# Optimization experiments

Hardware: AMD Instinct MI355X
Metric: run time of the kernel (lower is better)

The kernel has to match this reference:

```python
import jax, jax.numpy as jnp
import numpy as np

B, SEQ, TOK = 32, 200, 50
E, H, NHID, L = 512, 8, 2048, 6
DH = E // H
VOC, TC_EMB = 12525, 1024

def _make_mask(batch, heads, S):
    # True = masked. Heads 0-5: sliding window of size 10 unmasked.
    # Heads 6+: unmasked only for batch 0 (faithful to original code's indexing).
    # Row 0 (CLS) attends everywhere.
    m = np.ones((batch, heads, S, S), dtype=bool)
    j = np.arange(S)[:, None]
    cols = np.clip(j - 5 + np.arange(10)[None, :], 0, S - 1)
    rows = np.broadcast_to(j, cols.shape)
    local = np.ones((S, S), dtype=bool)
    local[rows.ravel(), cols.ravel()] = False
    m[:, :6] = local
    m[0, 6:] = False
    m[:, :, 0, :] = False
    return jnp.asarray(m)

MASK_101 = _make_mask(B, H, 101)
MASK_200 = _make_mask(B, H, 200)

def _layer_norm(x):
    mu = x.mean(-1, keepdims=True)
    sx = x - mu
    var = (sx * sx).mean(-1, keepdims=True)
    return sx * jax.lax.rsqrt(var + 1e-12)

def _ln_affine(x, g, b):
    return _layer_norm(x) * g + b

def _textcnn(ids, emb, cws, cbs, fw, fb):
    x = emb[ids][:, None, :, :]  # [N,1,50,1024] NCHW
    feats = []
    for w, b in zip(cws, cbs):
        y = jax.lax.conv_general_dilated(x, w, (1, 1), 'VALID',
                dimension_numbers=('NCHW', 'OIHW', 'NCHW'))
        y = jax.nn.relu(y + b[None, :, None, None])[..., 0]  # [N,100,T]
        feats.append(y.max(axis=2))
    return jnp.concatenate(feats, axis=1) @ fw.T + fb  # [N,512]

def _encoder(x, mask, Wq, bq, Wk, bk, Wv, bv, Wo, bo, W1, b1, W2, b2, g1, be1, g2, be2):
    scale = float(np.sqrt(DH))
    def heads(t):  # [B,S,E] -> [B,H,S,DH]
        return t.reshape(t.shape[0], t.shape[1], H, DH).transpose(0, 2, 1, 3)
    for l in range(L):
        q = x @ Wq[l].T + bq[l]
        k = x @ Wk[l].T + bk[l]
        v = x @ Wv[l].T + bv[l]
        scores = jnp.einsum('bhqd,bhkd->bhqk', heads(q), heads(k)) / scale
        attn = jax.nn.softmax(jnp.where(mask, -1e9, scores), axis=-1)
        ctx = jnp.einsum('bhqk,bhkd->bhqd', attn, heads(v))
        ctx = ctx.transpose(0, 2, 1, 3).reshape(x.shape[0], -1, E) @ Wo[l].T + bo[l]
        x = _ln_affine(x + ctx, g1[l], be1[l])
        ff = jax.nn.relu(x @ W1[l].T + b1[l]) @ W2[l].T + b2[l]
        x = _ln_affine(x + ff, g2[l], be2[l])
    return x


def reference(src, label_similarity, tc_emb, cw1, cb1, cw2, cb2, cw3, cb3,
              tc_fc_w, tc_fc_b, Wq, bq, Wk, bk, Wv, bv, Wo, bo,
              W1, b1, W2, b2, ln1_g, ln1_b, ln2_g, ln2_b,
              fc1_w, fc1_b, fc2_w, fc2_b, fc3_w, fc3_b, post_scale, post_bias):
    cws, cbs = (cw1, cw2, cw3), (cb1, cb2, cb3)
    enc = lambda x, m: _encoder(x, m, Wq, bq, Wk, bk, Wv, bv, Wo, bo,
                                W1, b1, W2, b2, ln1_g, ln1_b, ln2_g, ln2_b)

    def post(h, S):
        h = jax.nn.gelu(h @ fc1_w.T + fc1_b, approximate=False)
        h = _layer_norm(h)
        return h * post_scale[:, :S, :] + post_bias[:, :S, :]

    # branch 1: first 100 JDs + CLS
    x = _textcnn(src[:, :100, :].reshape(-1, TOK), tc_emb, cws, cbs, tc_fc_w, tc_fc_b)
    x = _layer_norm(x.reshape(B, 100, E))
    x = jnp.concatenate([jnp.zeros((B, 1, E), x.dtype), x], axis=1)  # [B,101,E]
    pred = post(enc(x, MASK_101), 101)
    pred = pred @ fc2_w.T + fc2_b  # [B,101,200]
    cls_e = pred[:, :1, :]  # [B,1,200]
    tok = pred[:, 1:, :].transpose(0, 2, 1) @ fc3_w.T + fc3_b  # [B,200,200]
    tok = jax.nn.softmax(label_similarity, axis=-1) + 0.4 * tok
    tok = jnp.einsum('bnm,bom->bn', tok, cls_e)  # [B,200]

    # branch 2: all 200 JDs
    y = _textcnn(src.reshape(-1, TOK), tc_emb, cws, cbs, tc_fc_w, tc_fc_b)
    y = _layer_norm(y.reshape(B, SEQ, E))
    all_pred = post(enc(y, MASK_200), SEQ)
    pred1 = all_pred @ fc2_w.T + fc2_b  # [B,200,200]

    nnb = SEQ // 100  # 2
    def seg_soft(t, i):  # faithful (quirky) slice t[:, i:(i+1)*100]
        return jax.nn.softmax(t[:, i:(i + 1) * 100, :].mean(axis=1), axis=-1)
    kl_rows, euc_rows = [], []
    for i in range(nnb):
        kr, er = [], []
        for j in range(nnb):
            c1 = seg_soft(pred1, i) + 1e-6
            c2 = seg_soft(pred1, j) + 1e-6
            a1 = seg_soft(all_pred, i) + 1e-6
            a2 = seg_soft(all_pred, j) + 1e-6
            kr.append((c1 * jnp.log(c1 / c2)).sum(-1))
            er.append(jnp.sqrt(jnp.maximum(((a1 - a2) ** 2).sum(-1), 1e-12)))
        kl_rows.append(jnp.stack(kr, -1))
        euc_rows.append(jnp.stack(er, -1))
    sims_kl = jax.nn.softmax(jnp.stack(kl_rows, 1).reshape(B, -1) * 10, axis=-1) + 1e-6
    sims_euc = jax.nn.softmax(jnp.stack(euc_rows, 1).reshape(B, -1), axis=-1) + 1e-6
    loss = (sims_kl * jnp.log(sims_kl / sims_euc)).sum(-1).mean() * 100000 * 0.2

    return (jax.nn.softmax(tok, axis=-1), jax.nn.softmax(cls_e, axis=-1), loss)


def setup_inputs():
    key = jax.random.key(0)
    ks = jax.random.split(key, 20)
    f = lambda k, s: jax.random.normal(k, s, jnp.float32) * 0.02
    emb = f(ks[0], (VOC, TC_EMB)).at[0].set(0.0)  # padding_idx=0
    return {
        'src': jax.random.randint(ks[1], (B, SEQ, TOK), 0, VOC),
        'label_similarity': jax.random.normal(ks[2], (200, 200), jnp.float32),
        'tc_emb': emb,
        'cw1': f(ks[3], (100, 1, 1, TC_EMB)), 'cb1': jnp.zeros((100,)),
        'cw2': f(ks[4], (100, 1, 2, TC_EMB)), 'cb2': jnp.zeros((100,)),
        'cw3': f(ks[5], (100, 1, 3, TC_EMB)), 'cb3': jnp.zeros((100,)),
        'tc_fc_w': f(ks[6], (E, 300)), 'tc_fc_b': jnp.zeros((E,)),
        'Wq': f(ks[7], (L, E, E)), 'bq': jnp.zeros((L, E)),
        'Wk': f(ks[8], (L, E, E)), 'bk': jnp.zeros((L, E)),
        'Wv': f(ks[9], (L, E, E)), 'bv': jnp.zeros((L, E)),
        'Wo': f(ks[10], (L, E, E)), 'bo': jnp.zeros((L, E)),
        'W1': f(ks[11], (L, NHID, E)), 'b1': jnp.zeros((L, NHID)),
        'W2': f(ks[12], (L, E, NHID)), 'b2': jnp.zeros((L, E)),
        'ln1_g': jnp.ones((L, E)), 'ln1_b': jnp.zeros((L, E)),
        'ln2_g': jnp.ones((L, E)), 'ln2_b': jnp.zeros((L, E)),
        'fc1_w': f(ks[13], (E, E)), 'fc1_b': jnp.zeros((E,)),
        'fc2_w': f(ks[14], (200, E)), 'fc2_b': jnp.zeros((200,)),
        'fc3_w': f(ks[15], (200, 100)), 'fc3_b': jnp.zeros((200,)),
        'post_scale': jnp.ones((B, 300, E)), 'post_bias': jnp.zeros((B, 300, E)),
    }
```

## Files before the change

kernel.cpp:

```cpp
#include <hip/hip_runtime.h>
#include <float.h>
#include <math.h>


#define B_   32
#define SEQ_ 200
#define TOK_ 50
#define E_   512
#define H_   8
#define DH_  64
#define NHID_ 2048
#define L_   6
#define VOC_ 12525
#define TCE_ 1024

typedef unsigned short ushort_t;
typedef __attribute__((ext_vector_type(8))) short bf16x8;
typedef __attribute__((ext_vector_type(4))) float f32x4;
typedef __attribute__((address_space(1))) const unsigned int GU32;
typedef __attribute__((address_space(3))) unsigned int LU32;

__device__ __forceinline__ unsigned short f2bf(float x){
  unsigned u = __float_as_uint(x);
  unsigned r = u + 0x7fff + ((u >> 16) & 1);
  return (unsigned short)(r >> 16);
}
__device__ __forceinline__ float bf2f(unsigned short h){
  return __uint_as_float(((unsigned)h) << 16);
}

__device__ __forceinline__ float waveReduceSum(float v){
#pragma unroll
  for (int o = 32; o > 0; o >>= 1) v += __shfl_down(v, o, 64);
  return v;
}
__device__ __forceinline__ float waveReduceMax(float v){
#pragma unroll
  for (int o = 32; o > 0; o >>= 1) v = fmaxf(v, __shfl_down(v, o, 64));
  return v;
}
__device__ __forceinline__ float blockReduceSum256(float v, float* sm){
  v = waveReduceSum(v);
  int lane = threadIdx.x & 63, w = threadIdx.x >> 6;
  __syncthreads();
  if (lane == 0) sm[w] = v;
  __syncthreads();
  return sm[0] + sm[1] + sm[2] + sm[3];
}
__device__ __forceinline__ float blockReduceMax256(float v, float* sm){
  v = waveReduceMax(v);
  int lane = threadIdx.x & 63, w = threadIdx.x >> 6;
  __syncthreads();
  if (lane == 0) sm[w] = v;
  __syncthreads();
  return fmaxf(fmaxf(sm[0], sm[1]), fmaxf(sm[2], sm[3]));
}

__global__ __launch_bounds__(256) void gemm_k(
    const float* __restrict__ A, const float* __restrict__ B,
    const float* __restrict__ bias, const float* __restrict__ Res,
    float* __restrict__ C,
    int M, int N, int K,
    long long sAm, long long sAk, long long sBn, long long sBk,
    long long sCm, long long sRm,
    int Hd,
    long long bAb, long long bAh, long long bBb, long long bBh,
    long long bCb, long long bCh,
    float alpha, int epi)
{
  __shared__ float As[16][68];
  __shared__ float Bs[16][68];
  int z = blockIdx.z;
  int zb = z / Hd, zh = z - zb * Hd;
  A += (long long)zb * bAb + (long long)zh * bAh;
  B += (long long)zb * bBb + (long long)zh * bBh;
  C += (long long)zb * bCb + (long long)zh * bCh;
  int m0 = blockIdx.y * 64, n0 = blockIdx.x * 64;
  int tid = threadIdx.y * 16 + threadIdx.x;
  float acc[4][4] = {};
  for (int k0 = 0; k0 < K; k0 += 16) {
#pragma unroll
    for (int i = 0; i < 4; ++i) {
      int idx = tid + 256 * i;
      int kk = idx & 15, mm = idx >> 4;
      int m = m0 + mm, k = k0 + kk;
      As[kk][mm] = (m < M && k < K) ? A[(long long)m * sAm + (long long)k * sAk] : 0.f;
      int n = n0 + mm;
      Bs[kk][mm] = (n < N && k < K) ? B[(long long)n * sBn + (long long)k * sBk] : 0.f;
    }
    __syncthreads();
#pragma unroll
    for (int kk = 0; kk < 16; ++kk) {
      float a[4], b[4];
#pragma unroll
      for (int i = 0; i < 4; ++i) a[i] = As[kk][threadIdx.y * 4 + i];
#pragma unroll
      for (int j = 0; j < 4; ++j) b[j] = Bs[kk][threadIdx.x * 4 + j];
#pragma unroll
      for (int i = 0; i < 4; ++i)
#pragma unroll
        for (int j = 0; j < 4; ++j) acc[i][j] = fmaf(a[i], b[j], acc[i][j]);
    }
    __syncthreads();
  }
#pragma unroll
  for (int i = 0; i < 4; ++i) {
    int m = m0 + threadIdx.y * 4 + i;
    if (m >= M) continue;
#pragma unroll
    for (int j = 0; j < 4; ++j) {
      int n = n0 + threadIdx.x * 4 + j;
      if (n >= N) continue;
      float v = acc[i][j] * alpha;
      if (bias) v += bias[n];
      if (epi == 1) v = fmaxf(v, 0.f);
      else if (epi == 2) v = 0.5f * v * (1.f + erff(v * 0.70710678f));
      if (Res) v += Res[(long long)m * sRm + n];
      C[(long long)m * sCm + n] = v;
    }
  }
}

static inline void launch_gemm(hipStream_t st,
    const float* A, const float* B, const float* bias, const float* Res, float* C,
    int M, int N, int K,
    long long sAm, long long sAk, long long sBn, long long sBk,
    long long sCm, long long sRm,
    int nz, int Hd,
    long long bAb, long long bAh, long long bBb, long long bBh,
    long long bCb, long long bCh,
    float alpha, int epi)
{
  dim3 g((N + 63) / 64, (M + 63) / 64, nz), bl(16, 16);
  gemm_k<<<g, bl, 0, st>>>(A, B, bias, Res, C, M, N, K,
                           sAm, sAk, sBn, sBk, sCm, sRm, Hd,
                           bAb, bAh, bBb, bBh, bCb, bCh, alpha, epi);
}

__global__ __launch_bounds__(256) void mgemm_k(
    const ushort_t* __restrict__ Ah, const ushort_t* __restrict__ Al,
    const ushort_t* __restrict__ Bh, const ushort_t* __restrict__ Bl,
    const float* __restrict__ bias, const float* __restrict__ Res,
    float* __restrict__ Cf, ushort_t* __restrict__ Chh, ushort_t* __restrict__ Cll,
    int M, int N, int K, int epi, int Mslice, int Nt, int nsplit,
    int kstepsPer, long long splitStride)
{
  __shared__ __align__(16) ushort_t smem[4][128 * 32];
  int lin = blockIdx.x;
  int xcd = lin & 7;
  int q = lin >> 3;
  int ml = q % Mslice;
  int q2 = q / Mslice;
  int nt = q2 % Nt;
  int sp = q2 / Nt;
  int mt = xcd * Mslice + ml;
  if (mt * 128 >= M) return;
  int m0 = mt * 128, n0 = nt * 128;
  int kbase = sp * kstepsPer;
  int tid = threadIdx.x;
  int lane = tid & 63, wv = tid >> 6;
  int wm = (wv >> 1) * 64, wn = (wv & 1) * 64;
  int fr = lane & 15, fq = lane >> 4;
  f32x4 acc[4][4];
  f32x4 zero = {0.f, 0.f, 0.f, 0.f};
#pragma unroll
  for (int i = 0; i < 4; ++i)
#pragma unroll
    for (int j = 0; j < 4; ++j) acc[i][j] = zero;

  for (int ks = 0; ks < kstepsPer; ++ks) {
    int k0 = (kbase + ks) << 5;
#pragma unroll
    for (int it = 0; it < 8; ++it) {
      int c = tid + it * 256;
      int buf = c >> 9;
      int cc = c & 511;
      int row = cc >> 2, cb = (cc & 3) * 8;
      const ushort_t* gsrc;
      long long grow;
      if (buf < 2) { int ar = m0 + row; if (ar >= M) ar = M - 1; grow = ar;
                     gsrc = buf ? Al : Ah; }
      else         { int br = n0 + row; if (br >= N) br = N - 1; grow = br;
                     gsrc = (buf == 2) ? Bh : Bl; }
      __builtin_amdgcn_global_load_lds((GU32*)(gsrc + grow * K + k0 + cb),
                                       (LU32*)(&smem[buf][0] + cc * 8), 16, 0, 0);
    }
    __syncthreads();
    bf16x8 ah[4], al[4], bh8[4], bl8[4];
#pragma unroll
    for (int i = 0; i < 4; ++i) {
      ah[i]  = *(const bf16x8*)(&smem[0][0] + (wm + i * 16 + fr) * 32 + fq * 8);
      al[i]  = *(const bf16x8*)(&smem[1][0] + (wm + i * 16 + fr) * 32 + fq * 8);
      bh8[i] = *(const bf16x8*)(&smem[2][0] + (wn + i * 16 + fr) * 32 + fq * 8);
      bl8[i] = *(const bf16x8*)(&smem[3][0] + (wn + i * 16 + fr) * 32 + fq * 8);
    }
#pragma unroll
    for (int i = 0; i < 4; ++i)
#pragma unroll
      for (int j = 0; j < 4; ++j) {
        acc[i][j] = __builtin_amdgcn_mfma_f32_16x16x32_bf16(ah[i], bh8[j], acc[i][j], 0, 0, 0);
        acc[i][j] = __builtin_amdgcn_mfma_f32_16x16x32_bf16(ah[i], bl8[j], acc[i][j], 0, 0, 0);
        acc[i][j] = __builtin_amdgcn_mfma_f32_16x16x32_bf16(al[i], bh8[j], acc[i][j], 0, 0, 0);
      }
    __syncthreads();
  }

  if (nsplit > 1) {
    float* Cs = Cf + (long long)sp * splitStride;
#pragma unroll
    for (int i = 0; i < 4; ++i)
#pragma unroll
      for (int j = 0; j < 4; ++j) {
        int col = n0 + wn + j * 16 + fr;
        if (col >= N) continue;
#pragma unroll
        for (int r = 0; r < 4; ++r) {
          int row = m0 + wm + i * 16 + fq * 4 + r;
          if (row >= M) continue;
          Cs[(long long)row * N + col] = acc[i][j][r];
        }
      }
    return;
  }
#pragma unroll
  for (int i = 0; i < 4; ++i) {
#pragma unroll
    for (int j = 0; j < 4; ++j) {
      int col = n0 + wn + j * 16 + fr;
      if (col >= N) continue;
#pragma unroll
      for (int r = 0; r < 4; ++r) {
        int row = m0 + wm + i * 16 + fq * 4 + r;
        if (row >= M) continue;
        float v = acc[i][j][r];
        if (bias) v += bias[col];
        if (epi == 1) v = fmaxf(v, 0.f);
        else if (epi == 2) v = 0.5f * v * (1.f + erff(v * 0.70710678f));
        long long idx = (long long)row * N + col;
        if (Res) v += Res[idx];
        if (Cf) Cf[idx] = v;
        if (Chh) {
          unsigned short h = f2bf(v);
          Chh[idx] = h;
          Cll[idx] = f2bf(v - bf2f(h));
        }
      }
    }
  }
}

__global__ void add_bias2_k(const float* __restrict__ s0, const float* __restrict__ s1,
                            const float* __restrict__ bias, float* __restrict__ o,
                            int total, int N){
  int idx = blockIdx.x * 256 + threadIdx.x;
  if (idx >= total) return;
  o[idx] = s0[idx] + s1[idx] + bias[idx % N];
}

__global__ void qkv_reduce_k(const float* __restrict__ s0, const float* __restrict__ s1,
                             const float* __restrict__ bias, float* __restrict__ o,
                             long long total){
  long long idx = ((long long)blockIdx.x * 256 + threadIdx.x) * 4;
  if (idx >= total) return;
  float4 a = *(const float4*)(s0 + idx);
  float4 b = *(const float4*)(s1 + idx);
  int c = (int)(idx % 1536);
  float4 bi = *(const float4*)(bias + c);
  float4 r;
  r.x = a.x + b.x + bi.x; r.y = a.y + b.y + bi.y;
  r.z = a.z + b.z + bi.z; r.w = a.w + b.w + bi.w;
  *(float4*)(o + idx) = r;
}

#define BND_ROWS 64
#define BND_STAGE 73
__global__ __launch_bounds__(256) void attn_band(
    const float* __restrict__ QKV,
    ushort_t* __restrict__ oh, ushort_t* __restrict__ ol, int S, int nrb)
{
  __shared__ float Kl[BND_STAGE][68];
  __shared__ float Vl[BND_STAGE][68];
  __shared__ float Ql[BND_ROWS][68];
  __shared__ float sc[BND_ROWS][12];
  int bh = blockIdx.x / nrb, rblk = blockIdx.x % nrb;
  int b = bh / 6, h = bh % 6;
  int r0 = 1 + rblk * BND_ROWS;
  int nrows = S - r0; if (nrows > BND_ROWS) nrows = BND_ROWS;
  int lo0 = r0 - 5; if (lo0 < 0) lo0 = 0;
  int hi0 = r0 + nrows - 1 + 4; if (hi0 > S - 1) hi0 = S - 1;
  int cnt = hi0 - lo0 + 1;
  int t = threadIdx.x;
  const float* base = QKV + ((long long)(b * S + lo0)) * 1536 + h * 64;
  for (int idx = t; idx < cnt * 64; idx += 256) {
    int row = idx >> 6, d = idx & 63;
    Kl[row][d] = base[(long long)row * 1536 + 512 + d];
    Vl[row][d] = base[(long long)row * 1536 + 1024 + d];
  }
  const float* qbase = QKV + ((long long)(b * S + r0)) * 1536 + h * 64;
  for (int idx = t; idx < nrows * 64; idx += 256) {
    int row = idx >> 6, d = idx & 63;
    Ql[row][d] = qbase[(long long)row * 1536 + d];
  }
  __syncthreads();
  for (int p = t; p < nrows * 10; p += 256) {
    int ri = p / 10, jo = p - ri * 10;
    int r = r0 + ri;
    int lo = r - 5; if (lo < 0) lo = 0;
    int hi = r + 4; if (hi > S - 1) hi = S - 1;
    int j = lo + jo;
    float s;
    if (j > hi) s = -FLT_MAX;
    else {
      int jl = j - lo0;
      float a = 0.f;
      const float4* qv = (const float4*)&Ql[ri][0];
      const float4* kv = (const float4*)&Kl[jl][0];
#pragma unroll
      for (int c = 0; c < 16; ++c) {
        float4 x = qv[c], y = kv[c];
        a += x.x * y.x + x.y * y.y + x.z * y.z + x.w * y.w;
      }
      s = a * 0.125f;
    }
    sc[ri][jo] = s;
  }
  __syncthreads();
  if (t < nrows) {
    float mx = -FLT_MAX;
#pragma unroll
    for (int jo = 0; jo < 10; ++jo) mx = fmaxf(mx, sc[t][jo]);
    float pv[10]; float sum = 0.f;
#pragma unroll
    for (int jo = 0; jo < 10; ++jo) {
      float s = sc[t][jo];
      float e = (s == -FLT_MAX) ? 0.f : expf(s - mx);
      pv[jo] = e; sum += e;
    }
    float inv = 1.f / sum;
#pragma unroll
    for (int jo = 0; jo < 10; ++jo) sc[t][jo] = pv[jo] * inv;
  }
  __syncthreads();
  for (int idx = t; idx < nrows * 64; idx += 256) {
    int ri = idx >> 6, d = idx & 63;
    int r = r0 + ri;
    int lo = r - 5; if (lo < 0) lo = 0;
    int jbase = lo - lo0;
    float a = 0.f;
#pragma unroll
    for (int jo = 0; jo < 10; ++jo) {
      int jl = jbase + jo; if (jl >= cnt) jl = cnt - 1;
      a += sc[ri][jo] * Vl[jl][d];
    }
    long long o = ((long long)(b * S + r)) * 512 + h * 64 + d;
    unsigned short hh = f2bf(a);
    oh[o] = hh; ol[o] = f2bf(a - bf2f(hh));
  }
}

__global__ __launch_bounds__(256) void attn_full(
    const float* __restrict__ QKV,
    ushort_t* __restrict__ oh, ushort_t* __restrict__ ol, int S)
{
  __shared__ float sm_m[4], sm_l[4], sm_acc[4][64];
  int idx = blockIdx.x;
  int b, h, i;
  if (idx < B_ * H_) { b = idx >> 3; h = idx & 7; i = 0; }
  else { int r = idx - B_ * H_; h = 6 + r / (S - 1); i = 1 + r % (S - 1); b = 0; }
  int t = threadIdx.x, lane = t & 63, w = t >> 6;
  const float* Qr = QKV + ((long long)(b * S + i)) * 1536 + h * 64;
  const float* Kb = QKV + ((long long)(b * S)) * 1536 + 512 + h * 64;
  const float* Vb = QKV + ((long long)(b * S)) * 1536 + 1024 + h * 64;
  float q = Qr[lane];
  float m = -FLT_MAX, l = 0.f, acc = 0.f;
  for (int j0 = w * 4; j0 < S; j0 += 16) {
    float s[4];
#pragma unroll
    for (int c = 0; c < 4; ++c) {
      int j = j0 + c;
      float kv = (j < S) ? Kb[(long long)j * 1536 + lane] : 0.f;
      float r = waveReduceSum(q * kv);
      s[c] = r * 0.125f;
    }
#pragma unroll
    for (int c = 0; c < 4; ++c) {
      s[c] = __shfl(s[c], 0);
      if (j0 + c >= S) s[c] = -FLT_MAX;
    }
    float mc = fmaxf(fmaxf(s[0], s[1]), fmaxf(s[2], s[3]));
    float mn = fmaxf(m, mc);
    float scale = (m == -FLT_MAX) ? 0.f : expf(m - mn);
    float lsum = 0.f, vsum = 0.f;
#pragma unroll
    for (int c = 0; c < 4; ++c) {
      int j = j0 + c;
      if (j < S) {
        float p = expf(s[c] - mn);
        lsum += p;
        vsum += p * Vb[(long long)j * 1536 + lane];
      }
    }
    acc = acc * scale + vsum;
    l = l * scale + lsum;
    m = mn;
  }
  sm_m[w] = m;
  sm_l[w] = l;
  sm_acc[w][lane] = acc;
  __syncthreads();
  if (t < 64) {
    float M = fmaxf(fmaxf(sm_m[0], sm_m[1]), fmaxf(sm_m[2], sm_m[3]));
    float L = 0.f, A = 0.f;
#pragma unroll
    for (int w2 = 0; w2 < 4; ++w2) {
      float e = (sm_m[w2] == -FLT_MAX) ? 0.f : expf(sm_m[w2] - M);
      L += sm_l[w2] * e;
      A += sm_acc[w2][t] * e;
    }
    float ctx = A / L;
    long long o = ((long long)(b * S + i)) * 512 + h * 64 + t;
    unsigned short hh = f2bf(ctx);
    oh[o] = hh; ol[o] = f2bf(ctx - bf2f(hh));
  }
}

__global__ __launch_bounds__(256) void attn_unif(
    const float* __restrict__ QKV,
    ushort_t* __restrict__ oh, ushort_t* __restrict__ ol, int S)
{
  __shared__ float part[4][64];
  __shared__ float vm[64];
  int blk = blockIdx.x;
  int b = 1 + (blk >> 1), h = 6 + (blk & 1);
  int t = threadIdx.x, lane = t & 63, w = t >> 6;
  const float* Vb = QKV + ((long long)(b * S)) * 1536 + 1024 + h * 64;
  float s = 0.f;
  for (int j = w; j < S; j += 4) s += Vb[(long long)j * 1536 + lane];
  part[w][lane] = s;
  __syncthreads();
  if (t < 64) vm[t] = (part[0][t] + part[1][t] + part[2][t] + part[3][t]) * (1.f / S);
  __syncthreads();
  float m = vm[lane];
  unsigned short hh = f2bf(m);
  unsigned short hl = f2bf(m - bf2f(hh));
  for (int i = 1 + w; i < S; i += 4) {
    long long o = ((long long)(b * S + i)) * 512 + h * 64 + lane;
    oh[o] = hh; ol[o] = hl;
  }
}

__global__ void conv_hl(const float* __restrict__ x, ushort_t* __restrict__ h,
                        ushort_t* __restrict__ l, long long n){
  long long i = (long long)blockIdx.x * 256 + threadIdx.x;
  if (i >= n) return;
  float v = x[i];
  unsigned short hh = f2bf(v);
  h[i] = hh;
  l[i] = f2bf(v - bf2f(hh));
}

__global__ void conv_qkv(const float* __restrict__ Wq, const float* __restrict__ Wk,
                         const float* __restrict__ Wv,
                         ushort_t* __restrict__ h, ushort_t* __restrict__ l){
  int idx = blockIdx.x * 256 + threadIdx.x;
  if (idx >= L_ * 1536 * 512) return;
  int li = idx / (1536 * 512);
  int r = (idx / 512) % 1536;
  int c = idx & 511;
  const float* W = (r < 512) ? Wq : (r < 1024) ? Wk : Wv;
  int rr = r & 511;
  float v = W[(long long)li * 262144 + rr * 512 + c];
  unsigned short hh = f2bf(v);
  h[idx] = hh;
  l[idx] = f2bf(v - bf2f(hh));
}

__global__ void pack_bqkv(const float* __restrict__ bq, const float* __restrict__ bk,
                          const float* __restrict__ bv, float* __restrict__ o){
  int idx = blockIdx.x * 256 + threadIdx.x;
  if (idx >= L_ * 1536) return;
  int l = idx / 1536, r = idx % 1536;
  o[idx] = (r < 512) ? bq[l * 512 + r] : (r < 1024) ? bk[l * 512 + r - 512]
                                                    : bv[l * 512 + r - 1024];
}

__global__ void build_tcfw_hl(const float* __restrict__ w,
                              ushort_t* __restrict__ h, ushort_t* __restrict__ l){
  int idx = blockIdx.x * 256 + threadIdx.x;
  if (idx >= 512 * 320) return;
  int r = idx / 320, c = idx - r * 320;
  float v = (c < 300) ? w[r * 300 + c] : 0.f;
  unsigned short hh = f2bf(v);
  h[idx] = hh;
  l[idx] = f2bf(v - bf2f(hh));
}

__global__ void build_wcat(const float* __restrict__ cw1, const float* __restrict__ cw2,
                           const float* __restrict__ cw3, float* __restrict__ w){
  int idx = blockIdx.x * 256 + threadIdx.x;
  if (idx >= 600 * 1024) return;
  int o = idx >> 10, c = idx & 1023;
  float v;
  if      (o < 100) v = cw1[o * 1024 + c];
  else if (o < 200) v = cw2[(o - 100) * 2048 + c];
  else if (o < 300) v = cw2[(o - 200) * 2048 + 1024 + c];
  else if (o < 400) v = cw3[(o - 300) * 3072 + c];
  else if (o < 500) v = cw3[(o - 400) * 3072 + 1024 + c];
  else              v = cw3[(o - 500) * 3072 + 2048 + c];
  w[idx] = v;
}

__global__ void build_wcat_hl(const float* __restrict__ cw1, const float* __restrict__ cw2,
                              const float* __restrict__ cw3,
                              ushort_t* __restrict__ wh, ushort_t* __restrict__ wl){
  int idx = blockIdx.x * 256 + threadIdx.x;
  if (idx >= 640 * 1024) return;
  int o = idx >> 10, c = idx & 1023;
  float v = 0.f;
  if      (o < 100) v = cw1[o * 1024 + c];
  else if (o < 200) v = cw2[(o - 100) * 2048 + c];
  else if (o < 300) v = cw2[(o - 200) * 2048 + 1024 + c];
  else if (o < 400) v = cw3[(o - 300) * 3072 + c];
  else if (o < 500) v = cw3[(o - 400) * 3072 + 1024 + c];
  else if (o < 600) v = cw3[(o - 500) * 3072 + 2048 + c];
  unsigned short h = f2bf(v);
  wh[idx] = h;
  wl[idx] = f2bf(v - bf2f(h));
}

__global__ void feats_k(const float* __restrict__ proj, const int* __restrict__ src,
                        const float* __restrict__ cb1, const float* __restrict__ cb2,
                        const float* __restrict__ cb3, float* __restrict__ feats, int ld){
  __shared__ int ids[TOK_];
  int n = blockIdx.x;
  int t = threadIdx.x;
  if (t < TOK_) ids[t] = src[n * TOK_ + t];
  __syncthreads();
  if (t >= 300) return;
  float bia, m = -FLT_MAX;
  if (t < 100) {
    bia = cb1[t];
    for (int k = 0; k < 50; ++k)
      m = fmaxf(m, proj[(long long)ids[k] * ld + t]);
  } else if (t < 200) {
    int o = t - 100; bia = cb2[o];
    for (int k = 0; k < 49; ++k)
      m = fmaxf(m, proj[(long long)ids[k] * ld + 100 + o] +
                   proj[(long long)ids[k + 1] * ld + 200 + o]);
  } else {
    int o = t - 200; bia = cb3[o];
    for (int k = 0; k < 48; ++k)
      m = fmaxf(m, proj[(long long)ids[k] * ld + 300 + o] +
                   proj[(long long)ids[k + 1] * ld + 400 + o] +
                   proj[(long long)ids[k + 2] * ld + 500 + o]);
  }
  feats[(long long)n * 300 + t] = fmaxf(m + bia, 0.f);
}

__global__ void feats_hl_k(const float* __restrict__ proj, const int* __restrict__ src,
                           const float* __restrict__ cb1, const float* __restrict__ cb2,
                           const float* __restrict__ cb3,
                           ushort_t* __restrict__ fh, ushort_t* __restrict__ fl, int ld){
  __shared__ int ids[TOK_];
  int n = blockIdx.x;
  int t = threadIdx.x;
  if (t < TOK_) ids[t] = src[n * TOK_ + t];
  __syncthreads();
  int region = t >> 7, col = t & 127;
  bool act = col < 100;
  bool pad = (region == 2) && (col >= 100) && (col < 120);
  float a = 0.f;
  if (act) {
    float bia, m = -FLT_MAX;
    if (region == 0) {
      bia = cb1[col];
      for (int k = 0; k < 50; ++k)
        m = fmaxf(m, proj[(long long)ids[k] * ld + col]);
    } else if (region == 1) {
      bia = cb2[col];
      for (int k = 0; k < 49; ++k)
        m = fmaxf(m, proj[(long long)ids[k] * ld + 100 + col] +
                     proj[(long long)ids[k + 1] * ld + 200 + col]);
    } else {
      bia = cb3[col];
      for (int k = 0; k < 48; ++k)
        m = fmaxf(m, proj[(long long)ids[k] * ld + 300 + col] +
                     proj[(long long)ids[k + 1] * ld + 400 + col] +
                     proj[(long long)ids[k + 2] * ld + 500 + col]);
    }
    a = fmaxf(m + bia, 0.f);
  }
  if (act || pad) {
    int outcol = region * 100 + col;
    long long o = (long long)n * 320 + outcol;
    unsigned short hh = f2bf(a);
    fh[o] = hh;
    fl[o] = f2bf(a - bf2f(hh));
  }
}

__global__ __launch_bounds__(256) void ln_k(
    const float* __restrict__ in, long long sstr, int nsplit,
    const float* __restrict__ bias2, const float* __restrict__ res2, int epi2,
    float* __restrict__ out, const float* __restrict__ g, const float* __restrict__ bta,
    ushort_t* __restrict__ oh, ushort_t* __restrict__ ol,
    const float* __restrict__ pscale, const float* __restrict__ pbias, int S)
{
  __shared__ float sm[4];
  long long row = blockIdx.x;
  int t = threadIdx.x;
  const float* x = in + row * E_;
  float v0 = x[t], v1 = x[t + 256];
  for (int s = 1; s < nsplit; ++s) {
    v0 += x[(long long)s * sstr + t];
    v1 += x[(long long)s * sstr + t + 256];
  }
  if (bias2) { v0 += bias2[t]; v1 += bias2[t + 256]; }
  if (epi2 == 1) { v0 = fmaxf(v0, 0.f); v1 = fmaxf(v1, 0.f); }
  else if (epi2 == 2) {
    v0 = 0.5f * v0 * (1.f + erff(v0 * 0.70710678f));
    v1 = 0.5f * v1 * (1.f + erff(v1 * 0.70710678f));
  }
  if (res2) { v0 += res2[row * E_ + t]; v1 += res2[row * E_ + t + 256]; }
  float* y = out + row * E_;
  float mu = blockReduceSum256(v0 + v1, sm) * (1.f / E_);
  float d0 = v0 - mu, d1 = v1 - mu;
  float var = blockReduceSum256(d0 * d0 + d1 * d1, sm) * (1.f / E_);
  float r = rsqrtf(var + 1e-12f);
  float o0 = d0 * r, o1 = d1 * r;
  if (g) { o0 = o0 * g[t] + bta[t]; o1 = o1 * g[t + 256] + bta[t + 256]; }
  if (pscale) {
    long long b = row / S, s = row % S;
    long long off = (b * 300 + s) * E_;
    o0 = o0 * pscale[off + t] + pbias[off + t];
    o1 = o1 * pscale[off + t + 256] + pbias[off + t + 256];
  }
  y[t] = o0; y[t + 256] = o1;
  if (oh) {
    unsigned short h0 = f2bf(o0), h1 = f2bf(o1);
    oh[row * E_ + t] = h0;       oh[row * E_ + t + 256] = h1;
    ol[row * E_ + t] = f2bf(o0 - bf2f(h0));
    ol[row * E_ + t + 256] = f2bf(o1 - bf2f(h1));
  }
}

__global__ void build_x1(const float* __restrict__ xln, float* __restrict__ x1){
  long long idx = (long long)blockIdx.x * 256 + threadIdx.x;
  if (idx >= 3232LL * 512) return;
  long long row = idx >> 9; int c = (int)(idx & 511);
  long long b = row / 101, s = row % 101;
  x1[idx] = (s == 0) ? 0.f : xln[((b * 200) + (s - 1)) * 512 + c];
}

__global__ __launch_bounds__(256) void attn_softmax(float* __restrict__ sc, int S){
  __shared__ float sm[4];
  long long row = blockIdx.x;
  int i = (int)(row % S); long long bh = row / S;
  int h = (int)(bh & 7); int b = (int)(bh >> 3);
  float* p = sc + row * S;
  int t = threadIdx.x;
  bool inr = t < S;
  bool allow;
  if (i == 0) allow = true;
  else if (h < 6) allow = (t >= i - 5) && (t <= i + 4);
  else allow = (b == 0);
  float v = inr ? (allow ? p[t] : -1e9f) : -FLT_MAX;
  float mx = blockReduceMax256(v, sm);
  float e = inr ? expf(v - mx) : 0.f;
  float s = blockReduceSum256(e, sm);
  if (inr) p[t] = e / s;
}

__global__ __launch_bounds__(256) void softmax_rows(const float* __restrict__ in,
                                                    float* __restrict__ out, int n){
  __shared__ float sm[4];
  long long row = blockIdx.x;
  const float* x = in + row * n;
  float* y = out + row * n;
  int t = threadIdx.x;
  float v0 = (t < n) ? x[t] : -FLT_MAX;
  float v1 = (t + 256 < n) ? x[t + 256] : -FLT_MAX;
  float mx = blockReduceMax256(fmaxf(v0, v1), sm);
  float e0 = (t < n) ? expf(v0 - mx) : 0.f;
  float e1 = (t + 256 < n) ? expf(v1 - mx) : 0.f;
  float s = blockReduceSum256(e0 + e1, sm);
  if (t < n) y[t] = e0 / s;
  if (t + 256 < n) y[t + 256] = e1 / s;
}

__global__ void copy_cls(const float* __restrict__ pred, float* __restrict__ cls){
  int idx = blockIdx.x * 256 + threadIdx.x;
  if (idx >= B_ * 200) return;
  int b = idx / 200, m = idx % 200;
  cls[idx] = pred[(long long)b * 101 * 200 + m];
}

__global__ __launch_bounds__(256) void tokvec_k(const float* __restrict__ lsoft,
                         const float* __restrict__ tokmat,
                         const float* __restrict__ cls, float* __restrict__ tv){
  __shared__ float sm[4];
  int bn = blockIdx.x; int b = bn / 200, n = bn % 200;
  int t = threadIdx.x;
  float s = 0.f;
  if (t < 200)
    s = (lsoft[n * 200 + t] + 0.4f * tokmat[((long long)b * 200 + n) * 200 + t]) * cls[b * 200 + t];
  float tot = blockReduceSum256(s, sm);
  if (t == 0) tv[bn] = tot;
}

__global__ __launch_bounds__(256) void seg_soft_k(const float* __restrict__ pred,
                         const float* __restrict__ allp,
                         float* __restrict__ c0, float* __restrict__ c1,
                         float* __restrict__ a0, float* __restrict__ a1){
  __shared__ float sm[4];
  int b = blockIdx.x, which = blockIdx.y;
  const float* srcp; int C;
  if (which < 2) { srcp = pred; C = 200; } else { srcp = allp; C = 512; }
  int i = which & 1;
  int start = i, cnt = i ? 199 : 100;
  float* dst = (which == 0) ? c0 : (which == 1) ? c1 : (which == 2) ? a0 : a1;
  const float* base = srcp + ((long long)b * 200 + start) * C;
  int t = threadIdx.x;
  float m0 = 0.f, m1 = 0.f;
  for (int r = 0; r < cnt; ++r) {
    if (t < C)       m0 += base[(long long)r * C + t];
    if (t + 256 < C) m1 += base[(long long)r * C + t + 256];
  }
  float inv = 1.f / cnt;
  m0 *= inv; m1 *= inv;
  float v0 = (t < C) ? m0 : -FLT_MAX;
  float v1 = (t + 256 < C) ? m1 : -FLT_MAX;
  float mx = blockReduceMax256(fmaxf(v0, v1), sm);
  float e0 = (t < C) ? expf(v0 - mx) : 0.f;
  float e1 = (t + 256 < C) ? expf(v1 - mx) : 0.f;
  float s = blockReduceSum256(e0 + e1, sm);
  if (t < C)       dst[(long long)b * C + t] = e0 / s;
  if (t + 256 < C) dst[(long long)b * C + t + 256] = e1 / s;
}

__global__ __launch_bounds__(256) void loss_partial_k(const float* __restrict__ c0,
                         const float* __restrict__ c1,
                         const float* __restrict__ a0, const float* __restrict__ a1,
                         float* __restrict__ partial){
  __shared__ float sm[4];
  int b = blockIdx.x, t = threadIdx.x;
  float k01 = 0.f, k10 = 0.f;
  if (t < 200) {
    float x = c0[b * 200 + t] + 1e-6f, y = c1[b * 200 + t] + 1e-6f;
    k01 = x * logf(x / y);
    k10 = y * logf(y / x);
  }
  float K01 = blockReduceSum256(k01, sm);
  float K10 = blockReduceSum256(k10, sm);
  float d0 = a0[b * 512 + t] - a1[b * 512 + t];
  float d1 = a0[b * 512 + t + 256] - a1[b * 512 + t + 256];
  float E2 = blockReduceSum256(d0 * d0 + d1 * d1, sm);
  if (t == 0) {
    float euc = sqrtf(fmaxf(E2, 1e-12f));
    float kv[4] = {0.f, K01 * 10.f, K10 * 10.f, 0.f};
    float ev[4] = {1e-6f, euc, euc, 1e-6f};
    float mk = fmaxf(fmaxf(kv[0], kv[1]), fmaxf(kv[2], kv[3]));
    float me = fmaxf(fmaxf(ev[0], ev[1]), fmaxf(ev[2], ev[3]));
    float sk = 0.f, se = 0.f;
    for (int q = 0; q < 4; ++q) { kv[q] = expf(kv[q] - mk); sk += kv[q];
                                  ev[q] = expf(ev[q] - me); se += ev[q]; }
    float p = 0.f;
    for (int q = 0; q < 4; ++q) {
      float aa = kv[q] / sk + 1e-6f, bb = ev[q] / se + 1e-6f;
      p += aa * logf(aa / bb);
    }
    partial[b] = p;
  }
}

__global__ void loss_final_k(const float* __restrict__ partial, float* __restrict__ out){
  if (threadIdx.x == 0) {
    float s = 0.f;
    for (int b = 0; b < B_; ++b) s += partial[b];
    out[0] = s * (100000.f * 0.2f / B_);
  }
}

extern "C" void kernel_launch(void* const* d_in, const int* in_sizes, int n_in,
                              void* d_out, int out_size, void* d_ws, size_t ws_size,
                              hipStream_t stream) {
  const int*   src   = (const int*)  d_in[0];
  const float* lab   = (const float*)d_in[1];
  const float* emb   = (const float*)d_in[2];
  const float* cw1   = (const float*)d_in[3];
  const float* cb1   = (const float*)d_in[4];
  const float* cw2   = (const float*)d_in[5];
  const float* cb2   = (const float*)d_in[6];
  const float* cw3   = (const float*)d_in[7];
  const float* cb3   = (const float*)d_in[8];
  const float* tcfw  = (const float*)d_in[9];
  const float* tcfb  = (const float*)d_in[10];
  const float* Wq    = (const float*)d_in[11];
  const float* bq    = (const float*)d_in[12];
  const float* Wk    = (const float*)d_in[13];
  const float* bk    = (const float*)d_in[14];
  const float* Wv    = (const float*)d_in[15];
  const float* bv    = (const float*)d_in[16];
  const float* Wo    = (const float*)d_in[17];
  const float* bo    = (const float*)d_in[18];
  const float* W1    = (const float*)d_in[19];
  const float* b1v   = (const float*)d_in[20];
  const float* W2    = (const float*)d_in[21];
  const float* b2v   = (const float*)d_in[22];
  const float* g1    = (const float*)d_in[23];
  const float* be1   = (const float*)d_in[24];
  const float* g2    = (const float*)d_in[25];
  const float* be2   = (const float*)d_in[26];
  const float* fc1w  = (const float*)d_in[27];
  const float* fc1b  = (const float*)d_in[28];
  const float* fc2w  = (const float*)d_in[29];
  const float* fc2b  = (const float*)d_in[30];
  const float* fc3w  = (const float*)d_in[31];
  const float* fc3b  = (const float*)d_in[32];
  const float* pscale= (const float*)d_in[33];
  const float* pbias = (const float*)d_in[34];
  float* out = (float*)d_out;
  float* ws  = (float*)d_ws;
  ushort_t* wsu = (ushort_t*)d_ws;

  const size_t NEED_MFMA = 215200000ULL;

  if (ws_size >= NEED_MFMA) {
    const long long P_EMBH  = 0;
    const long long P_EMBL  = 6412800;
    const long long P_WCATH = 12825600;
    const long long P_WCATL = 13153280;
    const long long P_PROJ  = 13480960;
    const long long P_FEATS = 21496960;
    const long long SZW4 = 6LL * 512 * 512;
    const long long SZW1 = 6LL * 2048 * 512;
    const long long UQKVH = 0;
    const long long UQKVL = 3 * SZW4;
    const long long UOH = 6 * SZW4, UOL = 7 * SZW4;
    const long long U1H = 8 * SZW4,            U1L = 8 * SZW4 + SZW1;
    const long long U2H = 8 * SZW4 + 2 * SZW1, U2L = 8 * SZW4 + 3 * SZW1;
    const long long UF1H = 8 * SZW4 + 4 * SZW1, UF1L = UF1H + 262144;
    const long long O_BIG  = 19136512;
    const long long O_XLN  = 32243712;
    const long long O_X1   = 35520512;
    const long long O_QKV  = 37175296;
    const long long O_TMP  = 47005696;
    const long long O_XH   = 50282496;
    const long long O_XL   = 51920896;
    const long long O_SM   = 53559296;
    const long long O_LSOFT= O_SM;
    const long long O_CLS  = O_LSOFT + 40000;
    const long long O_TV   = O_CLS + 6400;
    const long long O_C0   = O_TV + 6400;
    const long long O_C1   = O_C0 + 6400;
    const long long O_A0   = O_C1 + 6400;
    const long long O_A1   = O_A0 + 16384;
    const long long O_PART = O_A1 + 16384;
    const long long O_BQKV = O_PART + 64;
    const long long O_FC2W = O_BQKV + 9216;

    ushort_t* EMBH = (ushort_t*)(ws + P_EMBH);
    ushort_t* EMBL = (ushort_t*)(ws + P_EMBL);
    ushort_t* WCATH= (ushort_t*)(ws + P_WCATH);
    ushort_t* WCATL= (ushort_t*)(ws + P_WCATL);
    float* PROJ = ws + P_PROJ;
    ushort_t* FH = (ushort_t*)(ws + P_FEATS);
    ushort_t* FL = FH + 6400LL * 320;
    float* BIG  = ws + O_BIG;
    float* XLN  = ws + O_XLN;
    float* X1   = ws + O_X1;
    float* QKV  = ws + O_QKV;
    float* TMP  = ws + O_TMP;
    ushort_t* TCFWH = (ushort_t*)(ws + O_TMP);
    ushort_t* TCFWL = TCFWH + 512 * 320;
    ushort_t* XH = (ushort_t*)(ws + O_XH);
    ushort_t* XL = (ushort_t*)(ws + O_XL);
    float* LSOFT= ws + O_LSOFT;
    float* CLS  = ws + O_CLS;
    float* TV   = ws + O_TV;
    float* C0p  = ws + O_C0;
    float* C1p  = ws + O_C1;
    float* A0p  = ws + O_A0;
    float* A1p  = ws + O_A1;
    float* PART = ws + O_PART;
    float* BQKV = ws + O_BQKV;
    ushort_t* FC2WH = (ushort_t*)(ws + O_FC2W);
    ushort_t* FC2WL = FC2WH + 200 * 512;
    float* SPLIT = QKV;
    float* ALLP  = TMP;
    float* PRED  = QKV;
    float* FC2S  = QKV + 6553600;
    float* TOKMAT= QKV + 3276800;
    const long long QKV_SPLIT_STRIDE = O_BIG - O_QKV;

    auto mgemm = [&](const ushort_t* Ah, const ushort_t* Al,
                     const ushort_t* Bh, const ushort_t* Bl,
                     const float* bias, const float* Res, float* Cf,
                     ushort_t* Ch, ushort_t* Cl, int M, int N, int K, int epi,
                     int nsplit, long long splitStride){
      int Mt = (M + 127) / 128;
      int Nt = (N + 127) / 128;
      int Mslice = (Mt + 7) / 8;
      int kst = (K / nsplit) >> 5;
      dim3 g(8 * Mslice * Nt * nsplit);
      mgemm_k<<<g, 256, 0, stream>>>(Ah, Al, Bh, Bl, bias, Res, Cf, Ch, Cl,
                                     M, N, K, epi, Mslice, Nt, nsplit, kst, splitStride);
    };

    conv_hl<<<(VOC_ * TCE_ + 255) / 256, 256, 0, stream>>>(emb, EMBH, EMBL, (long long)VOC_ * TCE_);
    build_wcat_hl<<<(640 * 1024 + 255) / 256, 256, 0, stream>>>(cw1, cw2, cw3, WCATH, WCATL);
    mgemm(EMBH, EMBL, WCATH, WCATL, nullptr, nullptr, PROJ, nullptr, nullptr,
          VOC_, 640, TCE_, 0, 1, 0);
    feats_hl_k<<<B_ * SEQ_, 384, 0, stream>>>(PROJ, src, cb1, cb2, cb3, FH, FL, 640);
    build_tcfw_hl<<<(512 * 320 + 255) / 256, 256, 0, stream>>>(tcfw, TCFWH, TCFWL);
    mgemm(FH, FL, TCFWH, TCFWL, nullptr, nullptr, SPLIT, nullptr, nullptr,
          B_ * SEQ_, E_, 320, 0, 2, 6400LL * 512);
    ln_k<<<B_ * SEQ_, 256, 0, stream>>>(SPLIT, 6400LL * 512, 2, tcfb, nullptr, 0,
                                        XLN, nullptr, nullptr, nullptr, nullptr,
                                        nullptr, nullptr, SEQ_);
    build_x1<<<(3232 * 512 + 255) / 256, 256, 0, stream>>>(XLN, X1);

    conv_qkv<<<(L_ * 1536 * 512 + 255) / 256, 256, 0, stream>>>(Wq, Wk, Wv,
                                                                wsu + UQKVH, wsu + UQKVL);
    pack_bqkv<<<(L_ * 1536 + 255) / 256, 256, 0, stream>>>(bq, bk, bv, BQKV);
    conv_hl<<<(int)((SZW4 + 255) / 256), 256, 0, stream>>>(Wo, wsu + UOH, wsu + UOL, SZW4);
    conv_hl<<<(int)((SZW1 + 255) / 256), 256, 0, stream>>>(W1, wsu + U1H, wsu + U1L, SZW1);
    conv_hl<<<(int)((SZW1 + 255) / 256), 256, 0, stream>>>(W2, wsu + U2H, wsu + U2L, SZW1);
    conv_hl<<<(262144 + 255) / 256, 256, 0, stream>>>(fc1w, wsu + UF1H, wsu + UF1L, 262144);
    conv_hl<<<(200 * 512 + 255) / 256, 256, 0, stream>>>(fc2w, FC2WH, FC2WL, 200 * 512);

    auto encoder = [&](float* X, int S, int R){
      ushort_t* BIGH = (ushort_t*)BIG;
      ushort_t* BIGL = BIGH + (long long)R * NHID_;
      int nrb = (S - 1 + BND_ROWS - 1) / BND_ROWS;
      int nfull = B_ * H_ + 2 * (S - 1);
      long long sstr = (long long)R * E_;
      long long qtotal = (long long)R * 1536;
      for (int l = 0; l < L_; ++l) {
        long long oq = (long long)l * 1536 * 512;
        long long o4 = (long long)l * E_ * E_;
        long long o1 = (long long)l * NHID_ * E_;
        const float* bo_l = bo + l * E_;
        const float* b1_l = b1v + l * NHID_; const float* b2_l = b2v + l * E_;
        const float* g1_l = g1 + l * E_;  const float* be1_l = be1 + l * E_;
        const float* g2_l = g2 + l * E_;  const float* be2_l = be2 + l * E_;

        mgemm(XH, XL, wsu + UQKVH + oq, wsu + UQKVL + oq, nullptr,
              nullptr, QKV, nullptr, nullptr, R, 1536, E_, 0, 2, QKV_SPLIT_STRIDE);
        qkv_reduce_k<<<(int)((qtotal / 4 + 255) / 256), 256, 0, stream>>>(
            QKV, BIG, BQKV + l * 1536, QKV, qtotal);
        attn_band<<<B_ * 6 * nrb, 256, 0, stream>>>(QKV, XH, XL, S, nrb);
        attn_full<<<nfull, 256, 0, stream>>>(QKV, XH, XL, S);
        attn_unif<<<(B_ - 1) * 2, 256, 0, stream>>>(QKV, XH, XL, S);
        mgemm(XH, XL, wsu + UOH + o4, wsu + UOL + o4, nullptr, nullptr,
              SPLIT, nullptr, nullptr, R, E_, E_, 0, 4, sstr);
        ln_k<<<R, 256, 0, stream>>>(SPLIT, sstr, 4, bo_l, X, 0,
                                    X, g1_l, be1_l, XH, XL, nullptr, nullptr, S);
        mgemm(XH, XL, wsu + U1H + o1, wsu + U1L + o1, b1_l, nullptr, nullptr,
              BIGH, BIGL, R, NHID_, E_, 1 , 1, 0);
        mgemm(BIGH, BIGL, wsu + U2H + o1, wsu + U2L + o1, nullptr, nullptr,
              SPLIT, nullptr, nullptr, R, E_, NHID_, 0, 4, sstr);
        ln_k<<<R, 256, 0, stream>>>(SPLIT, sstr, 4, b2_l, X, 0,
                                    X, g2_l, be2_l, XH, XL, nullptr, nullptr, S);
      }
    };

    auto post = [&](int S, int R){
      long long sstr = (long long)R * E_;
      mgemm(XH, XL, wsu + UF1H, wsu + UF1L, nullptr, nullptr,
            SPLIT, nullptr, nullptr, R, E_, E_, 0, 4, sstr);
      ln_k<<<R, 256, 0, stream>>>(SPLIT, sstr, 4, fc1b, nullptr, 2 ,
                                  ALLP, nullptr, nullptr, XH, XL, pscale, pbias, S);
      mgemm(XH, XL, FC2WH, FC2WL, nullptr, nullptr, FC2S,
            nullptr, nullptr, R, 200, E_, 0, 2, (long long)R * 200);
      add_bias2_k<<<(R * 200 + 255) / 256, 256, 0, stream>>>(
          FC2S, FC2S + (long long)R * 200, fc2b, PRED, R * 200, 200);
    };

    conv_hl<<<((3232 * 512) + 255) / 256, 256, 0, stream>>>(X1, XH, XL, 3232LL * 512);
    encoder(X1, 101, B_ * 101);
    post(101, B_ * 101);
    copy_cls<<<(B_ * 200 + 255) / 256, 256, 0, stream>>>(PRED, CLS);
    softmax_rows<<<B_, 256, 0, stream>>>(CLS, out + 6400, 200);
    softmax_rows<<<200, 256, 0, stream>>>(lab, LSOFT, 200);
    launch_gemm(stream, PRED + 200, fc3w, fc3b, nullptr, TOKMAT, 200, 200, 100,
                1, 200, 100, 1, 200, 0,
                B_, 1, 101LL * 200, 0, 0, 0, 200LL * 200, 0, 1.f, 0);
    tokvec_k<<<B_ * 200, 256, 0, stream>>>(LSOFT, TOKMAT, CLS, TV);
    softmax_rows<<<B_, 256, 0, stream>>>(TV, out, 200);

    conv_hl<<<((6400 * 512) + 255) / 256, 256, 0, stream>>>(XLN, XH, XL, 6400LL * 512);
    encoder(XLN, SEQ_, B_ * SEQ_);
    post(SEQ_, B_ * SEQ_);
    {
      dim3 g(B_, 4);
      seg_soft_k<<<g, 256, 0, stream>>>(PRED, ALLP, C0p, C1p, A0p, A1p);
    }
    loss_partial_k<<<B_, 256, 0, stream>>>(C0p, C1p, A0p, A1p, PART);
    loss_final_k<<<1, 64, 0, stream>>>(PART, out + 12800);
    return;
  }

  const long long O_WCAT = 0;
  const long long O_PROJ = 614400;
  const long long O_FEATS= 8129400;
  const long long O_BIG  = 0;
  const long long O_XLN  = 13107200;
  const long long O_X1   = 16384000;
  const long long O_XQ   = 18038784;
  const long long O_XK   = 21315584;
  const long long O_XV   = 24592384;
  const long long O_CTX  = 27869184;
  const long long O_TMP  = 31145984;
  const long long O_SM   = 34422784;
  const long long O_LSOFT= O_SM;
  const long long O_CLS  = O_LSOFT + 40000;
  const long long O_TV   = O_CLS + 6400;
  const long long O_C0   = O_TV + 6400;
  const long long O_C1   = O_C0 + 6400;
  const long long O_A0   = O_C1 + 6400;
  const long long O_A1   = O_A0 + 16384;
  const long long O_PART = O_A1 + 16384;

  float* WCAT = ws + O_WCAT;
  float* PROJ = ws + O_PROJ;
  float* FEATS= ws + O_FEATS;
  float* BIG  = ws + O_BIG;
  float* XLN  = ws + O_XLN;
  float* X1   = ws + O_X1;
  float* XQ   = ws + O_XQ;
  float* XK   = ws + O_XK;
  float* XV   = ws + O_XV;
  float* CTX  = ws + O_CTX;
  float* TMP  = ws + O_TMP;
  float* LSOFT= ws + O_LSOFT;
  float* CLS  = ws + O_CLS;
  float* TV   = ws + O_TV;
  float* C0p  = ws + O_C0;
  float* C1p  = ws + O_C1;
  float* A0p  = ws + O_A0;
  float* A1p  = ws + O_A1;
  float* PART = ws + O_PART;

  build_wcat<<<(600 * 1024 + 255) / 256, 256, 0, stream>>>(cw1, cw2, cw3, WCAT);
  launch_gemm(stream, emb, WCAT, nullptr, nullptr, PROJ,
              VOC_, 600, TCE_, TCE_, 1, TCE_, 1, 600, 0,
              1, 1, 0,0,0,0,0,0, 1.f, 0);
  feats_k<<<B_ * SEQ_, 320, 0, stream>>>(PROJ, src, cb1, cb2, cb3, FEATS, 600);
  launch_gemm(stream, FEATS, tcfw, tcfb, nullptr, XLN,
              B_ * SEQ_, E_, 300, 300, 1, 300, 1, E_, 0,
              1, 1, 0,0,0,0,0,0, 1.f, 0);
  ln_k<<<B_ * SEQ_, 256, 0, stream>>>(XLN, 0, 1, nullptr, nullptr, 0,
                                      XLN, nullptr, nullptr, nullptr, nullptr,
                                      nullptr, nullptr, SEQ_);
  build_x1<<<(3232 * 512 + 255) / 256, 256, 0, stream>>>(XLN, X1);

  auto encoder = [&](float* X, int S, int R){
    for (int l = 0; l < L_; ++l) {
      const float* Wq_l = Wq + (long long)l * E_ * E_;
      const float* Wk_l = Wk + (long long)l * E_ * E_;
      const float* Wv_l = Wv + (long long)l * E_ * E_;
      const float* Wo_l = Wo + (long long)l * E_ * E_;
      const float* W1_l = W1 + (long long)l * NHID_ * E_;
      const float* W2_l = W2 + (long long)l * E_ * NHID_;
      const float* bq_l = bq + l * E_;  const float* bk_l = bk + l * E_;
      const float* bv_l = bv + l * E_;  const float* bo_l = bo + l * E_;
      const float* b1_l = b1v + l * NHID_; const float* b2_l = b2v + l * E_;
      const float* g1_l = g1 + l * E_;  const float* be1_l = be1 + l * E_;
      const float* g2_l = g2 + l * E_;  const float* be2_l = be2 + l * E_;

      launch_gemm(stream, X, Wq_l, bq_l, nullptr, XQ, R, E_, E_,
                  E_, 1, E_, 1, E_, 0, 1, 1, 0,0,0,0,0,0, 1.f, 0);
      launch_gemm(stream, X, Wk_l, bk_l, nullptr, XK, R, E_, E_,
                  E_, 1, E_, 1, E_, 0, 1, 1, 0,0,0,0,0,0, 1.f, 0);
      launch_gemm(stream, X, Wv_l, bv_l, nullptr, XV, R, E_, E_,
                  E_, 1, E_, 1, E_, 0, 1, 1, 0,0,0,0,0,0, 1.f, 0);
      launch_gemm(stream, XQ, XK, nullptr, nullptr, BIG, S, S, DH_,
                  E_, 1, E_, 1, S, 0,
                  B_ * H_, H_,
                  (long long)S * E_, DH_, (long long)S * E_, DH_,
                  (long long)H_ * S * S, (long long)S * S,
                  0.125f, 0);
      attn_softmax<<<B_ * H_ * S, 256, 0, stream>>>(BIG, S);
      launch_gemm(stream, BIG, XV, nullptr, nullptr, CTX, S, DH_, S,
                  S, 1, 1, E_, E_, 0,
                  B_ * H_, H_,
                  (long long)H_ * S * S, (long long)S * S,
                  (long long)S * E_, DH_,
                  (long long)S * E_, DH_,
                  1.f, 0);
      launch_gemm(stream, CTX, Wo_l, bo_l, X, TMP, R, E_, E_,
                  E_, 1, E_, 1, E_, E_, 1, 1, 0,0,0,0,0,0, 1.f, 0);
      ln_k<<<R, 256, 0, stream>>>(TMP, 0, 1, nullptr, nullptr, 0,
                                  X, g1_l, be1_l, nullptr, nullptr, nullptr, nullptr, S);
      launch_gemm(stream, X, W1_l, b1_l, nullptr, BIG, R, NHID_, E_,
                  E_, 1, E_, 1, NHID_, 0, 1, 1, 0,0,0,0,0,0, 1.f, 1);
      launch_gemm(stream, BIG, W2_l, b2_l, X, TMP, R, E_, NHID_,
                  NHID_, 1, NHID_, 1, E_, E_, 1, 1, 0,0,0,0,0,0, 1.f, 0);
      ln_k<<<R, 256, 0, stream>>>(TMP, 0, 1, nullptr, nullptr, 0,
                                  X, g2_l, be2_l, nullptr, nullptr, nullptr, nullptr, S);
    }
  };

  auto post = [&](float* X, int S, int R, float* H1v, float* ALLPf, float* PREDf){
    launch_gemm(stream, X, fc1w, fc1b, nullptr, H1v, R, E_, E_,
                E_, 1, E_, 1, E_, 0, 1, 1, 0,0,0,0,0,0, 1.f, 2);
    ln_k<<<R, 256, 0, stream>>>(H1v, 0, 1, nullptr, nullptr, 0,
                                ALLPf, nullptr, nullptr, nullptr, nullptr, pscale, pbias, S);
    launch_gemm(stream, ALLPf, fc2w, fc2b, nullptr, PREDf, R, 200, E_,
                E_, 1, E_, 1, 200, 0, 1, 1, 0,0,0,0,0,0, 1.f, 0);
  };

  encoder(X1, 101, B_ * 101);
  post(X1, 101, B_ * 101, XQ, XK, CTX);
  copy_cls<<<(B_ * 200 + 255) / 256, 256, 0, stream>>>(CTX, CLS);
  softmax_rows<<<B_, 256, 0, stream>>>(CLS, out + 6400, 200);
  softmax_rows<<<200, 256, 0, stream>>>(lab, LSOFT, 200);
  launch_gemm(stream, CTX + 200, fc3w, fc3b, nullptr, TMP, 200, 200, 100,
              1, 200, 100, 1, 200, 0,
              B_, 1, 101LL * 200, 0, 0, 0, 200LL * 200, 0, 1.f, 0);
  tokvec_k<<<B_ * 200, 256, 0, stream>>>(LSOFT, TMP, CLS, TV);
  softmax_rows<<<B_, 256, 0, stream>>>(TV, out, 200);

  encoder(XLN, SEQ_, B_ * SEQ_);
  post(XLN, SEQ_, B_ * SEQ_, XQ, XK, CTX);
  {
    dim3 g(B_, 4);
    seg_soft_k<<<g, 256, 0, stream>>>(CTX, XK, C0p, C1p, A0p, A1p);
  }
  loss_partial_k<<<B_, 256, 0, stream>>>(C0p, C1p, A0p, A1p, PART);
  loss_final_k<<<1, 64, 0, stream>>>(PART, out + 12800);
}
```

Baseline: 3.918 ms.

## Batch both encoder passes into one concatenated row stack sharing GEMMs

Concatenates the 101-token and 200-token sequences into one 9632-row activation buffer so each encoder layer runs its QKV, output, FFN and post-projection GEMMs once over both passes instead of twice. Attention kernels get a row offset so each sequence length is still handled separately. The QKV bias is fused into the GEMM epilogue, which drops the split-K reduce kernel. The FFN is split into two 1024-wide halves with accumulate-into-output split-K, which lets the workspace be repacked. The goal is fewer launches and better GPU fill on the smaller pass. The cost is a larger working set and in-place build_x1 aliasing.

```diff
diff --git a/kernel.cpp b/kernel.cpp
--- a/kernel.cpp
+++ b/kernel.cpp
@@ -13,6 +13,9 @@
 #define L_   6
 #define VOC_ 12525
 #define TCE_ 1024
+#define R1_  3232
+#define R2_  6400
+#define R3_  9632
 
 typedef unsigned short ushort_t;
 typedef __attribute__((ext_vector_type(8))) short bf16x8;
@@ -142,8 +145,8 @@
     const ushort_t* __restrict__ Bh, const ushort_t* __restrict__ Bl,
     const float* __restrict__ bias, const float* __restrict__ Res,
     float* __restrict__ Cf, ushort_t* __restrict__ Chh, ushort_t* __restrict__ Cll,
-    int M, int N, int K, int epi, int Mslice, int Nt, int nsplit,
-    int kstepsPer, long long splitStride)
+    int M, int N, int K, int ldB, int epi, int Mslice, int Nt, int nsplit,
+    int kstepsPer, long long splitStride, int accum)
 {
   __shared__ __align__(16) ushort_t smem[4][128 * 32];
   int lin = blockIdx.x;
@@ -177,12 +180,12 @@
       int cc = c & 511;
       int row = cc >> 2, cb = (cc & 3) * 8;
       const ushort_t* gsrc;
-      long long grow;
-      if (buf < 2) { int ar = m0 + row; if (ar >= M) ar = M - 1; grow = ar;
-                     gsrc = buf ? Al : Ah; }
-      else         { int br = n0 + row; if (br >= N) br = N - 1; grow = br;
-                     gsrc = (buf == 2) ? Bh : Bl; }
-      __builtin_amdgcn_global_load_lds((GU32*)(gsrc + grow * K + k0 + cb),
+      long long gaddr;
+      if (buf < 2) { int ar = m0 + row; if (ar >= M) ar = M - 1;
+                     gsrc = buf ? Al : Ah; gaddr = (long long)ar * K + k0 + cb; }
+      else         { int br = n0 + row; if (br >= N) br = N - 1;
+                     gsrc = (buf == 2) ? Bh : Bl; gaddr = (long long)br * ldB + k0 + cb; }
+      __builtin_amdgcn_global_load_lds((GU32*)(gsrc + gaddr),
                                        (LU32*)(&smem[buf][0] + cc * 8), 16, 0, 0);
     }
     __syncthreads();
@@ -217,7 +220,9 @@
         for (int r = 0; r < 4; ++r) {
           int row = m0 + wm + i * 16 + fq * 4 + r;
           if (row >= M) continue;
-          Cs[(long long)row * N + col] = acc[i][j][r];
+          long long idx = (long long)row * N + col;
+          if (accum) Cs[idx] += acc[i][j][r];
+          else       Cs[idx]  = acc[i][j][r];
         }
       }
     return;
@@ -257,26 +262,11 @@
   o[idx] = s0[idx] + s1[idx] + bias[idx % N];
 }
 
-__global__ void qkv_reduce_k(const float* __restrict__ s0, const float* __restrict__ s1,
-                             const float* __restrict__ bias, float* __restrict__ o,
-                             long long total){
-  long long idx = ((long long)blockIdx.x * 256 + threadIdx.x) * 4;
-  if (idx >= total) return;
-  float4 a = *(const float4*)(s0 + idx);
-  float4 b = *(const float4*)(s1 + idx);
-  int c = (int)(idx % 1536);
-  float4 bi = *(const float4*)(bias + c);
-  float4 r;
-  r.x = a.x + b.x + bi.x; r.y = a.y + b.y + bi.y;
-  r.z = a.z + b.z + bi.z; r.w = a.w + b.w + bi.w;
-  *(float4*)(o + idx) = r;
-}
-
 #define BND_ROWS 64
 #define BND_STAGE 73
 __global__ __launch_bounds__(256) void attn_band(
     const float* __restrict__ QKV,
-    ushort_t* __restrict__ oh, ushort_t* __restrict__ ol, int S, int nrb)
+    ushort_t* __restrict__ oh, ushort_t* __restrict__ ol, int S, int nrb, int row0)
 {
   __shared__ float Kl[BND_STAGE][68];
   __shared__ float Vl[BND_STAGE][68];
@@ -290,13 +280,13 @@
   int hi0 = r0 + nrows - 1 + 4; if (hi0 > S - 1) hi0 = S - 1;
   int cnt = hi0 - lo0 + 1;
   int t = threadIdx.x;
-  const float* base = QKV + ((long long)(b * S + lo0)) * 1536 + h * 64;
+  const float* base = QKV + ((long long)(row0 + b * S + lo0)) * 1536 + h * 64;
   for (int idx = t; idx < cnt * 64; idx += 256) {
     int row = idx >> 6, d = idx & 63;
     Kl[row][d] = base[(long long)row * 1536 + 512 + d];
     Vl[row][d] = base[(long long)row * 1536 + 1024 + d];
   }
-  const float* qbase = QKV + ((long long)(b * S + r0)) * 1536 + h * 64;
+  const float* qbase = QKV + ((long long)(row0 + b * S + r0)) * 1536 + h * 64;
   for (int idx = t; idx < nrows * 64; idx += 256) {
     int row = idx >> 6, d = idx & 63;
     Ql[row][d] = qbase[(long long)row * 1536 + d];
@@ -352,7 +342,7 @@
       int jl = jbase + jo; if (jl >= cnt) jl = cnt - 1;
       a += sc[ri][jo] * Vl[jl][d];
     }
-    long long o = ((long long)(b * S + r)) * 512 + h * 64 + d;
+    long long o = ((long long)(row0 + b * S + r)) * 512 + h * 64 + d;
     unsigned short hh = f2bf(a);
     oh[o] = hh; ol[o] = f2bf(a - bf2f(hh));
   }
@@ -360,7 +350,7 @@
 
 __global__ __launch_bounds__(256) void attn_full(
     const float* __restrict__ QKV,
-    ushort_t* __restrict__ oh, ushort_t* __restrict__ ol, int S)
+    ushort_t* __restrict__ oh, ushort_t* __restrict__ ol, int S, int row0)
 {
   __shared__ float sm_m[4], sm_l[4], sm_acc[4][64];
   int idx = blockIdx.x;
@@ -368,9 +358,9 @@
   if (idx < B_ * H_) { b = idx >> 3; h = idx & 7; i = 0; }
   else { int r = idx - B_ * H_; h = 6 + r / (S - 1); i = 1 + r % (S - 1); b = 0; }
   int t = threadIdx.x, lane = t & 63, w = t >> 6;
-  const float* Qr = QKV + ((long long)(b * S + i)) * 1536 + h * 64;
-  const float* Kb = QKV + ((long long)(b * S)) * 1536 + 512 + h * 64;
-  const float* Vb = QKV + ((long long)(b * S)) * 1536 + 1024 + h * 64;
+  const float* Qr = QKV + ((long long)(row0 + b * S + i)) * 1536 + h * 64;
+  const float* Kb = QKV + ((long long)(row0 + b * S)) * 1536 + 512 + h * 64;
+  const float* Vb = QKV + ((long long)(row0 + b * S)) * 1536 + 1024 + h * 64;
   float q = Qr[lane];
   float m = -FLT_MAX, l = 0.f, acc = 0.f;
   for (int j0 = w * 4; j0 < S; j0 += 16) {
@@ -418,7 +408,7 @@
       A += sm_acc[w2][t] * e;
     }
     float ctx = A / L;
-    long long o = ((long long)(b * S + i)) * 512 + h * 64 + t;
+    long long o = ((long long)(row0 + b * S + i)) * 512 + h * 64 + t;
     unsigned short hh = f2bf(ctx);
     oh[o] = hh; ol[o] = f2bf(ctx - bf2f(hh));
   }
@@ -426,14 +416,14 @@
 
 __global__ __launch_bounds__(256) void attn_unif(
     const float* __restrict__ QKV,
-    ushort_t* __restrict__ oh, ushort_t* __restrict__ ol, int S)
+    ushort_t* __restrict__ oh, ushort_t* __restrict__ ol, int S, int row0)
 {
   __shared__ float part[4][64];
   __shared__ float vm[64];
   int blk = blockIdx.x;
   int b = 1 + (blk >> 1), h = 6 + (blk & 1);
   int t = threadIdx.x, lane = t & 63, w = t >> 6;
-  const float* Vb = QKV + ((long long)(b * S)) * 1536 + 1024 + h * 64;
+  const float* Vb = QKV + ((long long)(row0 + b * S)) * 1536 + 1024 + h * 64;
   float s = 0.f;
   for (int j = w; j < S; j += 4) s += Vb[(long long)j * 1536 + lane];
   part[w][lane] = s;
@@ -444,7 +434,7 @@
   unsigned short hh = f2bf(m);
   unsigned short hl = f2bf(m - bf2f(hh));
   for (int i = 1 + w; i < S; i += 4) {
-    long long o = ((long long)(b * S + i)) * 512 + h * 64 + lane;
+    long long o = ((long long)(row0 + b * S + i)) * 512 + h * 64 + lane;
     oh[o] = hh; ol[o] = hl;
   }
 }
@@ -604,7 +594,8 @@
     const float* __restrict__ bias2, const float* __restrict__ res2, int epi2,
     float* __restrict__ out, const float* __restrict__ g, const float* __restrict__ bta,
     ushort_t* __restrict__ oh, ushort_t* __restrict__ ol,
-    const float* __restrict__ pscale, const float* __restrict__ pbias, int S)
+    const float* __restrict__ pscale, const float* __restrict__ pbias,
+    int S, long long bnd)
 {
   __shared__ float sm[4];
   long long row = blockIdx.x;
@@ -630,7 +621,11 @@
   float o0 = d0 * r, o1 = d1 * r;
   if (g) { o0 = o0 * g[t] + bta[t]; o1 = o1 * g[t + 256] + bta[t + 256]; }
   if (pscale) {
-    long long b = row / S, s = row % S;
+    long long b, s;
+    if (bnd >= 0) {
+      if (row < bnd) { b = row / 101; s = row % 101; }
+      else { long long rr = row - bnd; b = rr / 200; s = rr % 200; }
+    } else { b = row / S; s = row % S; }
     long long off = (b * 300 + s) * E_;
     o0 = o0 * pscale[off + t] + pbias[off + t];
     o1 = o1 * pscale[off + t + 256] + pbias[off + t + 256];
@@ -644,12 +639,12 @@
   }
 }
 
-__global__ void build_x1(const float* __restrict__ xln, float* __restrict__ x1){
+__global__ void build_x1(float* __restrict__ xc){
   long long idx = (long long)blockIdx.x * 256 + threadIdx.x;
-  if (idx >= 3232LL * 512) return;
+  if (idx >= (long long)R1_ * 512) return;
   long long row = idx >> 9; int c = (int)(idx & 511);
   long long b = row / 101, s = row % 101;
-  x1[idx] = (s == 0) ? 0.f : xln[((b * 200) + (s - 1)) * 512 + c];
+  xc[idx] = (s == 0) ? 0.f : xc[((long long)R1_ + b * 200 + (s - 1)) * 512 + c];
 }
 
 __global__ __launch_bounds__(256) void attn_softmax(float* __restrict__ sc, int S){
@@ -823,15 +818,9 @@
   float* ws  = (float*)d_ws;
   ushort_t* wsu = (ushort_t*)d_ws;
 
-  const size_t NEED_MFMA = 215200000ULL;
-
-  if (ws_size >= NEED_MFMA) {
-    const long long P_EMBH  = 0;
-    const long long P_EMBL  = 6412800;
-    const long long P_WCATH = 12825600;
-    const long long P_WCATL = 13153280;
-    const long long P_PROJ  = 13480960;
-    const long long P_FEATS = 21496960;
+  const size_t NEED_COMB = 215100000ULL;
+
+  if (ws_size >= NEED_COMB) {
     const long long SZW4 = 6LL * 512 * 512;
     const long long SZW1 = 6LL * 2048 * 512;
     const long long UQKVH = 0;
@@ -840,85 +829,73 @@
     const long long U1H = 8 * SZW4,            U1L = 8 * SZW4 + SZW1;
     const long long U2H = 8 * SZW4 + 2 * SZW1, U2L = 8 * SZW4 + 3 * SZW1;
     const long long UF1H = 8 * SZW4 + 4 * SZW1, UF1L = UF1H + 262144;
-    const long long O_BIG  = 19136512;
-    const long long O_XLN  = 32243712;
-    const long long O_X1   = 35520512;
-    const long long O_QKV  = 37175296;
-    const long long O_TMP  = 47005696;
-    const long long O_XH   = 50282496;
-    const long long O_XL   = 51920896;
-    const long long O_SM   = 53559296;
-    const long long O_LSOFT= O_SM;
-    const long long O_CLS  = O_LSOFT + 40000;
-    const long long O_TV   = O_CLS + 6400;
-    const long long O_C0   = O_TV + 6400;
-    const long long O_C1   = O_C0 + 6400;
-    const long long O_A0   = O_C1 + 6400;
-    const long long O_A1   = O_A0 + 16384;
-    const long long O_PART = O_A1 + 16384;
-    const long long O_BQKV = O_PART + 64;
-    const long long O_FC2W = O_BQKV + 9216;
-
-    ushort_t* EMBH = (ushort_t*)(ws + P_EMBH);
-    ushort_t* EMBL = (ushort_t*)(ws + P_EMBL);
-    ushort_t* WCATH= (ushort_t*)(ws + P_WCATH);
-    ushort_t* WCATL= (ushort_t*)(ws + P_WCATL);
-    float* PROJ = ws + P_PROJ;
-    ushort_t* FH = (ushort_t*)(ws + P_FEATS);
+    const long long O_W    = 0;
+    const long long O_QKV  = 19136512;
+    const long long O_BIG  = 33931264;
+    const long long O_XC   = 43794432;
+    const long long O_XHL  = 48726016;
+    const long long O_BQKV = 53657600;
+    const long long O_FC2W = 53666816;
+    ushort_t* EMBH = (ushort_t*)(ws + O_QKV);
+    ushort_t* EMBL = EMBH + (long long)VOC_ * TCE_;
+    ushort_t* WCATH= (ushort_t*)(ws + O_BIG);
+    ushort_t* WCATL= WCATH + 640 * 1024;
+    float* PROJ  = ws + O_BIG + 655360;
+    ushort_t* FH = (ushort_t*)(ws + O_QKV);
     ushort_t* FL = FH + 6400LL * 320;
-    float* BIG  = ws + O_BIG;
-    float* XLN  = ws + O_XLN;
-    float* X1   = ws + O_X1;
+    ushort_t* TCFWH = (ushort_t*)(ws + O_QKV + 2048000);
+    ushort_t* TCFWL = TCFWH + 512 * 320;
+    float* XALLS = ws + O_QKV + 2211840;
     float* QKV  = ws + O_QKV;
-    float* TMP  = ws + O_TMP;
-    ushort_t* TCFWH = (ushort_t*)(ws + O_TMP);
-    ushort_t* TCFWL = TCFWH + 512 * 320;
-    ushort_t* XH = (ushort_t*)(ws + O_XH);
-    ushort_t* XL = (ushort_t*)(ws + O_XL);
-    float* LSOFT= ws + O_LSOFT;
-    float* CLS  = ws + O_CLS;
-    float* TV   = ws + O_TV;
-    float* C0p  = ws + O_C0;
-    float* C1p  = ws + O_C1;
-    float* A0p  = ws + O_A0;
-    float* A1p  = ws + O_A1;
-    float* PART = ws + O_PART;
+    float* SPLIT= ws + O_QKV;
+    float* XC   = ws + O_XC;
+    ushort_t* XH = (ushort_t*)(ws + O_XHL);
+    ushort_t* XL = XH + (long long)R3_ * 512;
+    ushort_t* BIGH = (ushort_t*)(ws + O_BIG);
+    ushort_t* BIGL = BIGH + (long long)R3_ * 1024;
+    float* ALLP = ws + O_BIG;
     float* BQKV = ws + O_BQKV;
     ushort_t* FC2WH = (ushort_t*)(ws + O_FC2W);
     ushort_t* FC2WL = FC2WH + 200 * 512;
-    float* SPLIT = QKV;
-    float* ALLP  = TMP;
-    float* PRED  = QKV;
-    float* FC2S  = QKV + 6553600;
-    float* TOKMAT= QKV + 3276800;
-    const long long QKV_SPLIT_STRIDE = O_BIG - O_QKV;
+    float* FC2S  = ws + O_QKV + 9863168;
+    float* PRED  = ws + O_QKV;
+    float* TOKMAT= ws + O_QKV + 1926400;
+    float* CLS   = ws + O_QKV + 3206400;
+    float* TV    = ws + O_QKV + 3212800;
+    float* LSOFT = ws + O_QKV + 3219200;
+    float* C0p   = ws + O_QKV + 3259200;
+    float* C1p   = ws + O_QKV + 3265600;
+    float* A0p   = ws + O_QKV + 3272000;
+    float* A1p   = ws + O_QKV + 3288384;
+    float* PART  = ws + O_QKV + 3304768;
 
     auto mgemm = [&](const ushort_t* Ah, const ushort_t* Al,
-                     const ushort_t* Bh, const ushort_t* Bl,
+                     const ushort_t* Bh, const ushort_t* Bl, int ldB,
                      const float* bias, const float* Res, float* Cf,
                      ushort_t* Ch, ushort_t* Cl, int M, int N, int K, int epi,
-                     int nsplit, long long splitStride){
+                     int nsplit, long long splitStride, int accum){
       int Mt = (M + 127) / 128;
       int Nt = (N + 127) / 128;
       int Mslice = (Mt + 7) / 8;
       int kst = (K / nsplit) >> 5;
       dim3 g(8 * Mslice * Nt * nsplit);
       mgemm_k<<<g, 256, 0, stream>>>(Ah, Al, Bh, Bl, bias, Res, Cf, Ch, Cl,
-                                     M, N, K, epi, Mslice, Nt, nsplit, kst, splitStride);
+                                     M, N, K, ldB, epi, Mslice, Nt, nsplit,
+                                     kst, splitStride, accum);
     };
 
     conv_hl<<<(VOC_ * TCE_ + 255) / 256, 256, 0, stream>>>(emb, EMBH, EMBL, (long long)VOC_ * TCE_);
     build_wcat_hl<<<(640 * 1024 + 255) / 256, 256, 0, stream>>>(cw1, cw2, cw3, WCATH, WCATL);
-    mgemm(EMBH, EMBL, WCATH, WCATL, nullptr, nullptr, PROJ, nullptr, nullptr,
-          VOC_, 640, TCE_, 0, 1, 0);
+    mgemm(EMBH, EMBL, WCATH, WCATL, TCE_, nullptr, nullptr, PROJ, nullptr, nullptr,
+          VOC_, 640, TCE_, 0, 1, 0, 0);
     feats_hl_k<<<B_ * SEQ_, 384, 0, stream>>>(PROJ, src, cb1, cb2, cb3, FH, FL, 640);
     build_tcfw_hl<<<(512 * 320 + 255) / 256, 256, 0, stream>>>(tcfw, TCFWH, TCFWL);
-    mgemm(FH, FL, TCFWH, TCFWL, nullptr, nullptr, SPLIT, nullptr, nullptr,
-          B_ * SEQ_, E_, 320, 0, 2, 6400LL * 512);
-    ln_k<<<B_ * SEQ_, 256, 0, stream>>>(SPLIT, 6400LL * 512, 2, tcfb, nullptr, 0,
-                                        XLN, nullptr, nullptr, nullptr, nullptr,
-                                        nullptr, nullptr, SEQ_);
-    build_x1<<<(3232 * 512 + 255) / 256, 256, 0, stream>>>(XLN, X1);
+    mgemm(FH, FL, TCFWH, TCFWL, 320, nullptr, nullptr, XALLS, nullptr, nullptr,
+          R2_, E_, 320, 0, 2, 3276800LL, 0);
+    ln_k<<<R2_, 256, 0, stream>>>(XALLS, 3276800LL, 2, tcfb, nullptr, 0,
+                                  XC + (long long)R1_ * 512, nullptr, nullptr,
+                                  nullptr, nullptr, nullptr, nullptr, SEQ_, -1);
+    build_x1<<<(int)(((long long)R1_ * 512 + 255) / 256), 256, 0, stream>>>(XC);
 
     conv_qkv<<<(L_ * 1536 * 512 + 255) / 256, 256, 0, stream>>>(Wq, Wk, Wv,
                                                                 wsu + UQKVH, wsu + UQKVL);
@@ -929,57 +906,58 @@
     conv_hl<<<(262144 + 255) / 256, 256, 0, stream>>>(fc1w, wsu + UF1H, wsu + UF1L, 262144);
     conv_hl<<<(200 * 512 + 255) / 256, 256, 0, stream>>>(fc2w, FC2WH, FC2WL, 200 * 512);
 
-    auto encoder = [&](float* X, int S, int R){
-      ushort_t* BIGH = (ushort_t*)BIG;
-      ushort_t* BIGL = BIGH + (long long)R * NHID_;
-      int nrb = (S - 1 + BND_ROWS - 1) / BND_ROWS;
-      int nfull = B_ * H_ + 2 * (S - 1);
-      long long sstr = (long long)R * E_;
-      long long qtotal = (long long)R * 1536;
-      for (int l = 0; l < L_; ++l) {
-        long long oq = (long long)l * 1536 * 512;
-        long long o4 = (long long)l * E_ * E_;
-        long long o1 = (long long)l * NHID_ * E_;
-        const float* bo_l = bo + l * E_;
-        const float* b1_l = b1v + l * NHID_; const float* b2_l = b2v + l * E_;
-        const float* g1_l = g1 + l * E_;  const float* be1_l = be1 + l * E_;
-        const float* g2_l = g2 + l * E_;  const float* be2_l = be2 + l * E_;
-
-        mgemm(XH, XL, wsu + UQKVH + oq, wsu + UQKVL + oq, nullptr,
-              nullptr, QKV, nullptr, nullptr, R, 1536, E_, 0, 2, QKV_SPLIT_STRIDE);
-        qkv_reduce_k<<<(int)((qtotal / 4 + 255) / 256), 256, 0, stream>>>(
-            QKV, BIG, BQKV + l * 1536, QKV, qtotal);
-        attn_band<<<B_ * 6 * nrb, 256, 0, stream>>>(QKV, XH, XL, S, nrb);
-        attn_full<<<nfull, 256, 0, stream>>>(QKV, XH, XL, S);
-        attn_unif<<<(B_ - 1) * 2, 256, 0, stream>>>(QKV, XH, XL, S);
-        mgemm(XH, XL, wsu + UOH + o4, wsu + UOL + o4, nullptr, nullptr,
-              SPLIT, nullptr, nullptr, R, E_, E_, 0, 4, sstr);
-        ln_k<<<R, 256, 0, stream>>>(SPLIT, sstr, 4, bo_l, X, 0,
-                                    X, g1_l, be1_l, XH, XL, nullptr, nullptr, S);
-        mgemm(XH, XL, wsu + U1H + o1, wsu + U1L + o1, b1_l, nullptr, nullptr,
-              BIGH, BIGL, R, NHID_, E_, 1 , 1, 0);
-        mgemm(BIGH, BIGL, wsu + U2H + o1, wsu + U2L + o1, nullptr, nullptr,
-              SPLIT, nullptr, nullptr, R, E_, NHID_, 0, 4, sstr);
-        ln_k<<<R, 256, 0, stream>>>(SPLIT, sstr, 4, b2_l, X, 0,
-                                    X, g2_l, be2_l, XH, XL, nullptr, nullptr, S);
+    conv_hl<<<(int)(((long long)R3_ * 512 + 255) / 256), 256, 0, stream>>>(
+        XC, XH, XL, (long long)R3_ * 512);
+
+    const long long sstr = (long long)R3_ * 512;
+    const int nrb1 = (101 - 1 + BND_ROWS - 1) / BND_ROWS;
+    const int nrb2 = (200 - 1 + BND_ROWS - 1) / BND_ROWS;
+    const int nfull1 = B_ * H_ + 2 * (101 - 1);
+    const int nfull2 = B_ * H_ + 2 * (200 - 1);
+    for (int l = 0; l < L_; ++l) {
+      long long oq = (long long)l * 1536 * 512;
+      long long o4 = (long long)l * E_ * E_;
+      long long o1 = (long long)l * NHID_ * E_;
+      const float* bo_l = bo + l * E_;
+      const float* b1_l = b1v + l * NHID_; const float* b2_l = b2v + l * E_;
+      const float* g1_l = g1 + l * E_;  const float* be1_l = be1 + l * E_;
+      const float* g2_l = g2 + l * E_;  const float* be2_l = be2 + l * E_;
+
+      mgemm(XH, XL, wsu + UQKVH + oq, wsu + UQKVL + oq, 512, BQKV + l * 1536,
+            nullptr, QKV, nullptr, nullptr, R3_, 1536, E_, 0, 1, 0, 0);
+      attn_band<<<B_ * 6 * nrb1, 256, 0, stream>>>(QKV, XH, XL, 101, nrb1, 0);
+      attn_full<<<nfull1, 256, 0, stream>>>(QKV, XH, XL, 101, 0);
+      attn_unif<<<(B_ - 1) * 2, 256, 0, stream>>>(QKV, XH, XL, 101, 0);
+      attn_band<<<B_ * 6 * nrb2, 256, 0, stream>>>(QKV, XH, XL, 200, nrb2, R1_);
+      attn_full<<<nfull2, 256, 0, stream>>>(QKV, XH, XL, 200, R1_);
+      attn_unif<<<(B_ - 1) * 2, 256, 0, stream>>>(QKV, XH, XL, 200, R1_);
+      mgemm(XH, XL, wsu + UOH + o4, wsu + UOL + o4, 512, nullptr, nullptr,
+            SPLIT, nullptr, nullptr, R3_, E_, E_, 0, 2, sstr, 0);
+      ln_k<<<R3_, 256, 0, stream>>>(SPLIT, sstr, 2, bo_l, XC, 0,
+                                    XC, g1_l, be1_l, XH, XL, nullptr, nullptr, 0, -1);
+      for (int h = 0; h < 2; ++h) {
+        mgemm(XH, XL, wsu + U1H + o1 + (long long)h * 1024 * 512,
+              wsu + U1L + o1 + (long long)h * 1024 * 512, 512,
+              b1_l + h * 1024, nullptr, nullptr, BIGH, BIGL,
+              R3_, 1024, E_, 1 , 1, 0, 0);
+        mgemm(BIGH, BIGL, wsu + U2H + o1 + h * 1024,
+              wsu + U2L + o1 + h * 1024, 2048, nullptr, nullptr,
+              SPLIT, nullptr, nullptr, R3_, E_, 1024, 0, 2, sstr, h);
       }
-    };
-
-    auto post = [&](int S, int R){
-      long long sstr = (long long)R * E_;
-      mgemm(XH, XL, wsu + UF1H, wsu + UF1L, nullptr, nullptr,
-            SPLIT, nullptr, nullptr, R, E_, E_, 0, 4, sstr);
-      ln_k<<<R, 256, 0, stream>>>(SPLIT, sstr, 4, fc1b, nullptr, 2 ,
-                                  ALLP, nullptr, nullptr, XH, XL, pscale, pbias, S);
-      mgemm(XH, XL, FC2WH, FC2WL, nullptr, nullptr, FC2S,
-            nullptr, nullptr, R, 200, E_, 0, 2, (long long)R * 200);
-      add_bias2_k<<<(R * 200 + 255) / 256, 256, 0, stream>>>(
-          FC2S, FC2S + (long long)R * 200, fc2b, PRED, R * 200, 200);
-    };
-
-    conv_hl<<<((3232 * 512) + 255) / 256, 256, 0, stream>>>(X1, XH, XL, 3232LL * 512);
-    encoder(X1, 101, B_ * 101);
-    post(101, B_ * 101);
+      ln_k<<<R3_, 256, 0, stream>>>(SPLIT, sstr, 2, b2_l, XC, 0,
+                                    XC, g2_l, be2_l, XH, XL, nullptr, nullptr, 0, -1);
+    }
+
+    mgemm(XH, XL, wsu + UF1H, wsu + UF1L, 512, nullptr, nullptr,
+          SPLIT, nullptr, nullptr, R3_, E_, E_, 0, 2, sstr, 0);
+    ln_k<<<R3_, 256, 0, stream>>>(SPLIT, sstr, 2, fc1b, nullptr, 2 ,
+                                  ALLP, nullptr, nullptr, XH, XL,
+                                  pscale, pbias, 0, (long long)R1_);
+    mgemm(XH, XL, FC2WH, FC2WL, 512, nullptr, nullptr, FC2S,
+          nullptr, nullptr, R3_, 200, E_, 0, 2, (long long)R3_ * 200, 0);
+    add_bias2_k<<<(R3_ * 200 + 255) / 256, 256, 0, stream>>>(
+        FC2S, FC2S + (long long)R3_ * 200, fc2b, PRED, R3_ * 200, 200);
+
     copy_cls<<<(B_ * 200 + 255) / 256, 256, 0, stream>>>(PRED, CLS);
     softmax_rows<<<B_, 256, 0, stream>>>(CLS, out + 6400, 200);
     softmax_rows<<<200, 256, 0, stream>>>(lab, LSOFT, 200);
@@ -988,13 +966,11 @@
                 B_, 1, 101LL * 200, 0, 0, 0, 200LL * 200, 0, 1.f, 0);
     tokvec_k<<<B_ * 200, 256, 0, stream>>>(LSOFT, TOKMAT, CLS, TV);
     softmax_rows<<<B_, 256, 0, stream>>>(TV, out, 200);
-
-    conv_hl<<<((6400 * 512) + 255) / 256, 256, 0, stream>>>(XLN, XH, XL, 6400LL * 512);
-    encoder(XLN, SEQ_, B_ * SEQ_);
-    post(SEQ_, B_ * SEQ_);
     {
       dim3 g(B_, 4);
-      seg_soft_k<<<g, 256, 0, stream>>>(PRED, ALLP, C0p, C1p, A0p, A1p);
+      seg_soft_k<<<g, 256, 0, stream>>>(PRED + (long long)R1_ * 200,
+                                        ALLP + (long long)R1_ * 512,
+                                        C0p, C1p, A0p, A1p);
     }
     loss_partial_k<<<B_, 256, 0, stream>>>(C0p, C1p, A0p, A1p, PART);
     loss_final_k<<<1, 64, 0, stream>>>(PART, out + 12800);
@@ -1004,7 +980,7 @@
   const long long O_WCAT = 0;
   const long long O_PROJ = 614400;
   const long long O_FEATS= 8129400;
-  const long long O_BIG  = 0;
+  const long long O_BIGf = 0;
   const long long O_XLN  = 13107200;
   const long long O_X1   = 16384000;
   const long long O_XQ   = 18038784;
@@ -1025,7 +1001,7 @@
   float* WCAT = ws + O_WCAT;
   float* PROJ = ws + O_PROJ;
   float* FEATS= ws + O_FEATS;
-  float* BIG  = ws + O_BIG;
+  float* BIG  = ws + O_BIGf;
   float* XLN  = ws + O_XLN;
   float* X1   = ws + O_X1;
   float* XQ   = ws + O_XQ;
@@ -1052,8 +1028,13 @@
               1, 1, 0,0,0,0,0,0, 1.f, 0);
   ln_k<<<B_ * SEQ_, 256, 0, stream>>>(XLN, 0, 1, nullptr, nullptr, 0,
                                       XLN, nullptr, nullptr, nullptr, nullptr,
-                                      nullptr, nullptr, SEQ_);
-  build_x1<<<(3232 * 512 + 255) / 256, 256, 0, stream>>>(XLN, X1);
+                                      nullptr, nullptr, SEQ_, -1);
+  {
+  }
+  {
+  }
+  extern __global__ void build_x1_sep(const float*, float*);
+  build_x1_sep<<<(int)((3232LL * 512 + 255) / 256), 256, 0, stream>>>(XLN, X1);
 
   auto encoder = [&](float* X, int S, int R){
     for (int l = 0; l < L_; ++l) {
@@ -1092,13 +1073,13 @@
       launch_gemm(stream, CTX, Wo_l, bo_l, X, TMP, R, E_, E_,
                   E_, 1, E_, 1, E_, E_, 1, 1, 0,0,0,0,0,0, 1.f, 0);
       ln_k<<<R, 256, 0, stream>>>(TMP, 0, 1, nullptr, nullptr, 0,
-                                  X, g1_l, be1_l, nullptr, nullptr, nullptr, nullptr, S);
+                                  X, g1_l, be1_l, nullptr, nullptr, nullptr, nullptr, S, -1);
       launch_gemm(stream, X, W1_l, b1_l, nullptr, BIG, R, NHID_, E_,
                   E_, 1, E_, 1, NHID_, 0, 1, 1, 0,0,0,0,0,0, 1.f, 1);
       launch_gemm(stream, BIG, W2_l, b2_l, X, TMP, R, E_, NHID_,
                   NHID_, 1, NHID_, 1, E_, E_, 1, 1, 0,0,0,0,0,0, 1.f, 0);
       ln_k<<<R, 256, 0, stream>>>(TMP, 0, 1, nullptr, nullptr, 0,
-                                  X, g2_l, be2_l, nullptr, nullptr, nullptr, nullptr, S);
+                                  X, g2_l, be2_l, nullptr, nullptr, nullptr, nullptr, S, -1);
     }
   };
 
@@ -1106,7 +1087,8 @@
     launch_gemm(stream, X, fc1w, fc1b, nullptr, H1v, R, E_, E_,
                 E_, 1, E_, 1, E_, 0, 1, 1, 0,0,0,0,0,0, 1.f, 2);
     ln_k<<<R, 256, 0, stream>>>(H1v, 0, 1, nullptr, nullptr, 0,
-                                ALLPf, nullptr, nullptr, nullptr, nullptr, pscale, pbias, S);
+                                ALLPf, nullptr, nullptr, nullptr, nullptr,
+                                pscale, pbias, S, -1);
     launch_gemm(stream, ALLPf, fc2w, fc2b, nullptr, PREDf, R, 200, E_,
                 E_, 1, E_, 1, 200, 0, 1, 1, 0,0,0,0,0,0, 1.f, 0);
   };
@@ -1131,3 +1113,11 @@
   loss_partial_k<<<B_, 256, 0, stream>>>(C0p, C1p, A0p, A1p, PART);
   loss_final_k<<<1, 64, 0, stream>>>(PART, out + 12800);
 }
+
+__global__ void build_x1_sep(const float* __restrict__ xln, float* __restrict__ x1){
+  long long idx = (long long)blockIdx.x * 256 + threadIdx.x;
+  if (idx >= 3232LL * 512) return;
+  long long row = idx >> 9; int c = (int)(idx & 511);
+  long long b = row / 101, s = row % 101;
+  x1[idx] = (s == 0) ? 0.f : xln[((b * 200) + (s - 1)) * 512 + c];
+}
```

Measured after the change: 4.072 ms. 1.04x slower.
